# Optimization experiments

Measured on AMD Instinct MI355X. Metric: run time of the kernel, lower is better.

The kernel has to match this reference:

```python
import jax, jax.numpy as jnp
import numpy as np

D = 256; NH = 8; HD = D // NH; FF = 1024; NLAYERS = 6
REG_MAX = 32; NBIN = REG_MAX + 1; NC = 80; KQ = 4
SPATIAL = [(80, 80), (40, 40), (20, 20)]; NPTS = [4, 4, 4]; SUMP = sum(NPTS)
LQ = 300; B = 16; OFFSET_SCALE = 0.5; UP = 0.5; REG_SCALE = 4.0
TOT = NH * SUMP


def _project_np():
    ub1 = abs(UP) * abs(REG_SCALE); ub2 = ub1 * 2
    step = (ub1 + 1.0) ** (2.0 / (REG_MAX - 2))
    left = [-(step ** i) + 1 for i in range(REG_MAX // 2 - 1, 0, -1)]
    right = [step ** i - 1 for i in range(1, REG_MAX // 2)]
    return np.array([-ub2] + left + [0.0] + right + [ub2], dtype=np.float32)

PROJ_NP = _project_np()  # [NBIN]


def layer_norm(x, g, b):
    mu = x.mean(-1, keepdims=True)
    var = ((x - mu) ** 2).mean(-1, keepdims=True)
    return (x - mu) * jax.lax.rsqrt(var + 1e-5) * g + b


def inv_sigmoid(x, eps=1e-5):
    x = jnp.clip(x, eps, 1.0 - eps)
    return jnp.log(x) - jnp.log1p(-x)


def mlp2(x, w1, b1, w2, b2):
    return jax.nn.silu(x @ w1 + b1) @ w2 + b2


def mlp3(x, w1, b1, w2, b2, w3, b3):
    return jax.nn.silu(jax.nn.silu(x @ w1 + b1) @ w2 + b2) @ w3 + b3


def grid_sample(img, grid):
    # bilinear, padding_mode='zeros', align_corners=False. img [N,C,H,W], grid [N,Hg,Wg,2] in [-1,1]
    N, C, H, W = img.shape
    gshape = grid.shape[1:3]
    x = (grid[..., 0] + 1.0) * (W * 0.5) - 0.5
    y = (grid[..., 1] + 1.0) * (H * 0.5) - 0.5
    x0f = jnp.floor(x); y0f = jnp.floor(y)
    wx = x - x0f; wy = y - y0f
    x0 = x0f.astype(jnp.int32); y0 = y0f.astype(jnp.int32)
    imgf = img.reshape(N, C, H * W)
    def tap(xi, yi, wt):
        valid = ((xi >= 0) & (xi < W) & (yi >= 0) & (yi < H)).astype(img.dtype)
        idx = jnp.clip(yi, 0, H - 1) * W + jnp.clip(xi, 0, W - 1)
        v = jnp.take_along_axis(imgf, idx.reshape(N, 1, -1), axis=2).reshape(N, C, gshape[0], gshape[1])
        return v * (valid * wt)[:, None]
    return (tap(x0, y0, (1 - wx) * (1 - wy)) + tap(x0 + 1, y0, wx * (1 - wy))
            + tap(x0, y0 + 1, (1 - wx) * wy) + tap(x0 + 1, y0 + 1, wx * wy))


def self_attention(q_in, k_in, v_in, qw, qb, kw, kb, vw, vb, ow, ob):
    q = (q_in @ qw + qb).reshape(B, LQ, NH, HD)
    k = (k_in @ kw + kb).reshape(B, LQ, NH, HD)
    v = (v_in @ vw + vb).reshape(B, LQ, NH, HD)
    a = jax.nn.softmax(jnp.einsum('bqhd,bkhd->bhqk', q, k) * (HD ** -0.5), -1)
    o = jnp.einsum('bhqk,bkhd->bqhd', a, v).reshape(B, LQ, D)
    return o @ ow + ob


def distance2bbox(points, distance):
    rs = abs(REG_SCALE); half = 0.5 * rs
    x1 = points[..., 0] - (half + distance[..., 0]) * (points[..., 2] / rs)
    y1 = points[..., 1] - (half + distance[..., 1]) * (points[..., 3] / rs)
    x2 = points[..., 0] + (half + distance[..., 2]) * (points[..., 2] / rs)
    y2 = points[..., 1] + (half + distance[..., 3]) * (points[..., 3] / rs)
    return jnp.stack([(x1 + x2) * 0.5, (y1 + y2) * 0.5, x2 - x1, y2 - y1], -1)


def lqe_head(scores, corners, w1, b1, w2, b2):
    prob = jax.nn.softmax(corners.reshape(B, LQ, 4, NBIN), -1)
    topk, _ = jax.lax.top_k(prob, KQ)                         # [B,LQ,4,KQ]
    stat = jnp.concatenate([topk, topk.mean(-1, keepdims=True)], -1)  # [B,LQ,4,KQ+1]
    return scores + mlp2(stat.reshape(B, LQ, 4 * (KQ + 1)), w1, b1, w2, b2)


def reference(target, ref_pts_unact, memory,
              sa_qw, sa_qb, sa_kw, sa_kb, sa_vw, sa_vb, sa_ow, sa_ob,
              n1_g, n1_b, off_w, off_b, aw_w, aw_b,
              gate_w, gate_b, gn_g, gn_b,
              ff1_w, ff1_b, ff2_w, ff2_b, n3_g, n3_b,
              bb_w1, bb_b1, bb_w2, bb_b2, bb_w3, bb_b3,
              sc_w, sc_b, lqe_w1, lqe_b1, lqe_w2, lqe_b2,
              qp_w1, qp_b1, qp_w2, qp_b2,
              pb_w1, pb_b1, pb_w2, pb_b2, pb_w3, pb_b3):
    project = jnp.asarray(PROJ_NP)
    # --- value prep: memory [B,S,D] -> per-level [B*NH, HD, h, w] ---
    val = memory.reshape(B, -1, NH, HD).transpose(0, 2, 3, 1).reshape(B * NH, HD, -1)
    splits = np.cumsum([h * w for h, w in SPATIAL])[:-1].tolist()
    value_lvls = [v.reshape(B * NH, HD, h, w)
                  for v, (h, w) in zip(jnp.split(val, splits, axis=2), SPATIAL)]
    nps = jnp.asarray(np.repeat(1.0 / np.array(NPTS, np.float32), NPTS))  # [SUMP]

    ref_pts = jax.nn.sigmoid(ref_pts_unact)
    output = target
    out_prev = jnp.zeros_like(target)
    corners_prev = jnp.zeros((B, LQ, 4 * NBIN), dtype=target.dtype)
    ref_init = ref_pts
    final_logits = final_bboxes = None

    for i in range(NLAYERS):
        qp = jnp.clip(mlp2(ref_pts, qp_w1, qp_b1, qp_w2, qp_b2), -10.0, 10.0)
        # self attention
        q = output + qp
        t2 = self_attention(q, q, output, sa_qw[i], sa_qb[i], sa_kw[i], sa_kb[i],
                            sa_vw[i], sa_vb[i], sa_ow[i], sa_ob[i])
        output = layer_norm(output + t2, n1_g[i], n1_b[i])
        # deformable cross attention
        qc = output + qp
        offs = (qc @ off_w[i] + off_b[i]).reshape(B, LQ, NH, SUMP, 2)
        attnw = jax.nn.softmax((qc @ aw_w[i] + aw_b[i]).reshape(B, LQ, NH, SUMP), -1)
        offset = offs * nps[:, None] * ref_pts[:, :, None, None, 2:] * OFFSET_SCALE
        locs = ref_pts[:, :, None, None, :2] + offset            # [B,LQ,NH,SUMP,2]
        grids = (2.0 * locs - 1.0).transpose(0, 2, 1, 3, 4).reshape(B * NH, LQ, SUMP, 2)
        p0 = 0; sampled = []
        for lvl in range(len(SPATIAL)):
            sampled.append(grid_sample(value_lvls[lvl], grids[:, :, p0:p0 + NPTS[lvl]]))
            p0 += NPTS[lvl]
        samp = jnp.concatenate(sampled, -1)                      # [B*NH, HD, LQ, SUMP]
        aw = attnw.transpose(0, 2, 1, 3).reshape(B * NH, 1, LQ, SUMP)
        t2 = (samp * aw).sum(-1).reshape(B, D, LQ).transpose(0, 2, 1)
        # gateway
        g12 = jax.nn.sigmoid(jnp.concatenate([output, t2], -1) @ gate_w[i] + gate_b[i])
        output = layer_norm(g12[..., :D] * output + g12[..., D:] * t2, gn_g[i], gn_b[i])
        # FFN
        t2 = jax.nn.relu(output @ ff1_w[i] + ff1_b[i]) @ ff2_w[i] + ff2_b[i]
        output = layer_norm(jnp.clip(output + t2, -65504.0, 65504.0), n3_g[i], n3_b[i])
        # FDR box refinement
        if i == 0:
            pre_bb = jax.nn.sigmoid(mlp3(output, pb_w1, pb_b1, pb_w2, pb_b2, pb_w3, pb_b3)
                                    + inv_sigmoid(ref_pts))
            ref_init = pre_bb
        corners = mlp3(output + out_prev, bb_w1[i], bb_b1[i], bb_w2[i], bb_b2[i],
                       bb_w3[i], bb_b3[i]) + corners_prev
        dist = jax.nn.softmax(corners.reshape(B, LQ, 4, NBIN), -1) @ project  # [B,LQ,4]
        inter = distance2bbox(ref_init, dist)
        if i == NLAYERS - 1:  # eval_idx
            scores = output @ sc_w[i] + sc_b[i]
            final_logits = lqe_head(scores, corners, lqe_w1[i], lqe_b1[i], lqe_w2[i], lqe_b2[i])
            final_bboxes = inter
        corners_prev = corners
        ref_pts = inter
        out_prev = output
    return jnp.concatenate([final_bboxes, final_logits], -1)  # [B, LQ, 4+NC]


def setup_inputs() -> dict:
    key = jax.random.key(0)
    cnt = [0]
    def rnd(shape, scale=0.02):
        cnt[0] += 1
        return jax.random.normal(jax.random.fold_in(key, cnt[0]), shape, dtype=jnp.float32) * scale
    S = sum(h * w for h, w in SPATIAL)
    L = NLAYERS
    return {
        'target': rnd((B, LQ, D), 1.0),
        'ref_pts_unact': rnd((B, LQ, 4), 1.0),
        'memory': rnd((B, S, D), 1.0),
        'sa_qw': rnd((L, D, D)), 'sa_qb': rnd((L, D)),
        'sa_kw': rnd((L, D, D)), 'sa_kb': rnd((L, D)),
        'sa_vw': rnd((L, D, D)), 'sa_vb': rnd((L, D)),
        'sa_ow': rnd((L, D, D)), 'sa_ob': rnd((L, D)),
        'n1_g': jnp.ones((L, D)), 'n1_b': jnp.zeros((L, D)),
        'off_w': rnd((L, D, TOT * 2)), 'off_b': rnd((L, TOT * 2)),
        'aw_w': rnd((L, D, TOT)), 'aw_b': rnd((L, TOT)),
        'gate_w': rnd((L, 2 * D, 2 * D)), 'gate_b': rnd((L, 2 * D)),
        'gn_g': jnp.ones((L, D)), 'gn_b': jnp.zeros((L, D)),
        'ff1_w': rnd((L, D, FF)), 'ff1_b': rnd((L, FF)),
        'ff2_w': rnd((L, FF, D)), 'ff2_b': rnd((L, D)),
        'n3_g': jnp.ones((L, D)), 'n3_b': jnp.zeros((L, D)),
        'bb_w1': rnd((L, D, D)), 'bb_b1': rnd((L, D)),
        'bb_w2': rnd((L, D, D)), 'bb_b2': rnd((L, D)),
        'bb_w3': rnd((L, D, 4 * NBIN)), 'bb_b3': rnd((L, 4 * NBIN)),
        'sc_w': rnd((L, D, NC)), 'sc_b': rnd((L, NC)),
        'lqe_w1': rnd((L, 4 * (KQ + 1), 64)), 'lqe_b1': rnd((L, 64)),
        'lqe_w2': rnd((L, 64, 1)), 'lqe_b2': rnd((L, 1)),
        'qp_w1': rnd((4, 2 * D)), 'qp_b1': rnd((2 * D,)),
        'qp_w2': rnd((2 * D, D)), 'qp_b2': rnd((D,)),
        'pb_w1': rnd((D, D)), 'pb_b1': rnd((D,)),
        'pb_w2': rnd((D, D)), 'pb_b2': rnd((D,)),
        'pb_w3': rnd((D, 4)), 'pb_b3': rnd((4,)),
    }
```

## Files before the change

### kernel.cpp

```cpp
#include <hip/hip_runtime.h>
#include <cstddef>
#include <cmath>
#include <utility>

#define B_ 16
#define LQ_ 300
#define D_ 256
#define NH_ 8
#define HD_ 32
#define FF_ 1024
#define NBIN_ 33
#define NC_ 80
#define SUMP_ 12
#define TOT_ (NH_*SUMP_)
#define STOT_ 8400
#define R_ (B_*LQ_)
#define NLAYERS_ 6

typedef short bf16x8 __attribute__((ext_vector_type(8)));
typedef float f32x4  __attribute__((ext_vector_type(4)));

static __device__ __forceinline__ short f2bf(float x) {
  union { float f; unsigned u; } v; v.f = x;
  unsigned r = v.u + 0x7fffu + ((v.u >> 16) & 1u);
  return (short)(r >> 16);
}
static __device__ __forceinline__ float bf2f(short s) {
  union { unsigned u; float f; } v; v.u = ((unsigned)(unsigned short)s) << 16; return v.f;
}

__launch_bounds__(256)
__global__ void wconv_kernel(const float* __restrict__ W, short* __restrict__ Wt,
                             int K, int N, size_t ostride) {
  __shared__ float t[32][33];
  const float* Wl = W + (size_t)blockIdx.z * K * N;
  short* Wtl = Wt + (size_t)blockIdx.z * ostride;
  int k0 = blockIdx.x * 32, n0 = blockIdx.y * 32;
  int tr = threadIdx.x >> 5, tc = threadIdx.x & 31;
  #pragma unroll
  for (int i = 0; i < 4; ++i) {
    int k = k0 + tr + i * 8, n = n0 + tc;
    t[tr + i * 8][tc] = (k < K && n < N) ? Wl[(size_t)k * N + n] : 0.f;
  }
  __syncthreads();
  #pragma unroll
  for (int i = 0; i < 4; ++i) {
    int n = n0 + tr + i * 8, k = k0 + tc;
    if (n < N && k < K) Wtl[(size_t)n * K + k] = f2bf(t[tc][tr + i * 8]);
  }
}

__launch_bounds__(256)
__global__ void memconv_kernel(const float* __restrict__ mem, short* __restrict__ mb) {
  int gs = blockIdx.x * 4 + (threadIdx.x >> 6);
  int c  = (threadIdx.x & 63) * 4;
  int b = gs / STOT_, s = gs - b * STOT_;
  float4 v = *(const float4*)(mem + (size_t)gs * 256 + c);
  int h = c >> 5, cc = c & 31;
  short4 o; o.x = f2bf(v.x); o.y = f2bf(v.y); o.z = f2bf(v.z); o.w = f2bf(v.w);
  *(short4*)(mb + (((size_t)(b * 8 + h) * STOT_ + s) * 32) + cc) = o;
}

template<int ACT, int KT>
__launch_bounds__(256)
__global__ void bgemm(const short* __restrict__ A, const short* __restrict__ A2, int N2,
                      const short* __restrict__ Acat, int KA,
                      const short* __restrict__ Wt, const float* __restrict__ bias,
                      const float* __restrict__ Cadd, float* __restrict__ Cf,
                      short* __restrict__ Cbf, int M, int N) {
  const int bm = blockIdx.y * 64, bn = blockIdx.x * 64;
  const int tid = threadIdx.x, wid = tid >> 6, lane = tid & 63;
  const int wm = (wid >> 1) * 32, wn = (wid & 1) * 32;
  const int lr = lane & 15, lq = lane >> 4;
  const short* Ab = (A2 && bn >= N2) ? A2 : A;
  const int lda = Acat ? KA : KT;
  const int ldb = KT - KA;
  const int r0 = bm + wm + lr, r1 = r0 + 16;
  const int n0 = bn + wn + lr, n1 = n0 + 16;
  const bool v0 = n0 < N, v1 = n1 < N;
  const short* w0p = Wt + (size_t)(v0 ? n0 : 0) * KT + lq * 8;
  const short* w1p = Wt + (size_t)(v1 ? n1 : 0) * KT + lq * 8;
  f32x4 acc[2][2];
  #pragma unroll
  for (int i = 0; i < 2; ++i)
    #pragma unroll
    for (int j = 0; j < 2; ++j) acc[i][j] = (f32x4){0.f, 0.f, 0.f, 0.f};

  #pragma unroll 4
  for (int k0 = 0; k0 < KT; k0 += 32) {
    const short* src; int ko, ld;
    if (Acat && k0 >= KA) { src = Acat; ko = k0 - KA; ld = ldb; }
    else                  { src = Ab;   ko = k0;      ld = lda; }
    bf16x8 a0 = *(const bf16x8*)(src + (size_t)r0 * ld + ko + lq * 8);
    bf16x8 a1 = *(const bf16x8*)(src + (size_t)r1 * ld + ko + lq * 8);
    bf16x8 w0 = *(const bf16x8*)(w0p + k0);
    bf16x8 w1 = *(const bf16x8*)(w1p + k0);
    acc[0][0] = __builtin_amdgcn_mfma_f32_16x16x32_bf16(a0, w0, acc[0][0], 0, 0, 0);
    acc[0][1] = __builtin_amdgcn_mfma_f32_16x16x32_bf16(a0, w1, acc[0][1], 0, 0, 0);
    acc[1][0] = __builtin_amdgcn_mfma_f32_16x16x32_bf16(a1, w0, acc[1][0], 0, 0, 0);
    acc[1][1] = __builtin_amdgcn_mfma_f32_16x16x32_bf16(a1, w1, acc[1][1], 0, 0, 0);
  }
  #pragma unroll
  for (int ti = 0; ti < 2; ++ti)
    #pragma unroll
    for (int tj = 0; tj < 2; ++tj) {
      int gn = bn + wn + tj * 16 + lr;
      if (gn >= N) continue;
      float bv = bias[gn];
      #pragma unroll
      for (int r = 0; r < 4; ++r) {
        int gm = bm + wm + ti * 16 + lq * 4 + r;
        size_t idx = (size_t)gm * N + gn;
        float v = acc[ti][tj][r] + bv;
        if (Cadd) v += Cadd[idx];
        if (ACT == 1) v = fmaxf(v, 0.f);
        if (ACT == 2) v = v / (1.f + __expf(-v));
        if (ACT == 3) v = 1.f / (1.f + __expf(-v));
        if (ACT == 4) v = fminf(fmaxf(v, -10.f), 10.f);
        if (Cf)  Cf[idx] = v;
        if (Cbf) Cbf[idx] = f2bf(v);
      }
    }
}

template<int KT, int MODE>
__launch_bounds__(256)
__global__ void gemm_ln(const short* __restrict__ A, const short* __restrict__ Wt,
                        const float* __restrict__ bias, const float* __restrict__ resid,
                        const float* __restrict__ gamma, const float* __restrict__ beta,
                        const float* __restrict__ qp, float* __restrict__ prev,
                        float* __restrict__ outf, short* __restrict__ outbf,
                        short* __restrict__ oqbf) {
  __shared__ float ssum[16][4];
  __shared__ float ssq[16][4];
  const int m0 = blockIdx.x * 16;
  const int tid = threadIdx.x, wid = tid >> 6, lane = tid & 63;
  const int lr = lane & 15, lq = lane >> 4;
  const int arow = m0 + lr;
  const int cw = wid * 64;
  f32x4 acc[4];
  #pragma unroll
  for (int t = 0; t < 4; ++t) acc[t] = (f32x4){0.f, 0.f, 0.f, 0.f};
  #pragma unroll 4
  for (int k0 = 0; k0 < KT; k0 += 32) {
    bf16x8 a = *(const bf16x8*)(A + (size_t)arow * KT + k0 + lq * 8);
    #pragma unroll
    for (int t = 0; t < 4; ++t) {
      bf16x8 w = *(const bf16x8*)(Wt + (size_t)(cw + t * 16 + lr) * KT + k0 + lq * 8);
      acc[t] = __builtin_amdgcn_mfma_f32_16x16x32_bf16(a, w, acc[t], 0, 0, 0);
    }
  }
  float s[4] = {0.f, 0.f, 0.f, 0.f}, q[4] = {0.f, 0.f, 0.f, 0.f};
  #pragma unroll
  for (int t = 0; t < 4; ++t) {
    int col = cw + t * 16 + lr;
    float bv = bias[col];
    #pragma unroll
    for (int rr = 0; rr < 4; ++rr) {
      int rowg = m0 + lq * 4 + rr;
      float x = acc[t][rr] + bv + resid[(size_t)rowg * 256 + col];
      if (MODE == 1) x = fminf(fmaxf(x, -65504.f), 65504.f);
      acc[t][rr] = x;
      s[rr] += x; q[rr] += x * x;
    }
  }
  #pragma unroll
  for (int m = 1; m < 16; m <<= 1)
    #pragma unroll
    for (int rr = 0; rr < 4; ++rr) { s[rr] += __shfl_xor(s[rr], m); q[rr] += __shfl_xor(q[rr], m); }
  if (lr == 0)
    #pragma unroll
    for (int rr = 0; rr < 4; ++rr) {
      ssum[lq * 4 + rr][wid] = s[rr];
      ssq[lq * 4 + rr][wid] = q[rr];
    }
  __syncthreads();
  float mu[4], rs[4];
  #pragma unroll
  for (int rr = 0; rr < 4; ++rr) {
    int rl = lq * 4 + rr;
    float sm = ssum[rl][0] + ssum[rl][1] + ssum[rl][2] + ssum[rl][3];
    float sq = ssq[rl][0] + ssq[rl][1] + ssq[rl][2] + ssq[rl][3];
    float m_ = sm * (1.f / 256.f);
    float var = sq * (1.f / 256.f) - m_ * m_;
    mu[rr] = m_; rs[rr] = rsqrtf(var + 1e-5f);
  }
  #pragma unroll
  for (int t = 0; t < 4; ++t) {
    int col = cw + t * 16 + lr;
    float g = gamma[col], be = beta[col];
    #pragma unroll
    for (int rr = 0; rr < 4; ++rr) {
      int rowg = m0 + lq * 4 + rr;
      size_t idx = (size_t)rowg * 256 + col;
      float v = (acc[t][rr] - mu[rr]) * rs[rr] * g + be;
      outf[idx] = v;
      outbf[idx] = f2bf(v);
      if (MODE == 0) {
        oqbf[idx] = f2bf(v + qp[idx]);
      } else {
        float po = prev[idx];
        oqbf[idx] = f2bf(v + po);
        prev[idx] = v;
      }
    }
  }
}

__launch_bounds__(256)
__global__ void ffn_ln(const short* __restrict__ A, const short* __restrict__ W1t,
                       const float* __restrict__ b1, const short* __restrict__ W2t,
                       const float* __restrict__ b2, const float* __restrict__ resid,
                       const float* __restrict__ gamma, const float* __restrict__ beta,
                       float* __restrict__ prev, float* __restrict__ outf,
                       short* __restrict__ outbf, short* __restrict__ oqbf) {
  __shared__ short hid[16][1032];
  __shared__ float ssum[16][4];
  __shared__ float ssq[16][4];
  const int m0 = blockIdx.x * 16;
  const int tid = threadIdx.x, wid = tid >> 6, lane = tid & 63;
  const int lr = lane & 15, lq = lane >> 4;
  const int arow = m0 + lr;
  {
    f32x4 acc[16];
    #pragma unroll
    for (int t = 0; t < 16; ++t) acc[t] = (f32x4){0.f, 0.f, 0.f, 0.f};
    #pragma unroll 2
    for (int k0 = 0; k0 < 256; k0 += 32) {
      bf16x8 a = *(const bf16x8*)(A + (size_t)arow * 256 + k0 + lq * 8);
      #pragma unroll
      for (int t = 0; t < 16; ++t) {
        bf16x8 w = *(const bf16x8*)(W1t + (size_t)(wid * 256 + t * 16 + lr) * 256 + k0 + lq * 8);
        acc[t] = __builtin_amdgcn_mfma_f32_16x16x32_bf16(a, w, acc[t], 0, 0, 0);
      }
    }
    #pragma unroll
    for (int t = 0; t < 16; ++t) {
      int col = wid * 256 + t * 16 + lr;
      float bv = b1[col];
      #pragma unroll
      for (int rr = 0; rr < 4; ++rr)
        hid[lq * 4 + rr][col] = f2bf(fmaxf(acc[t][rr] + bv, 0.f));
    }
  }
  __syncthreads();
  const int cw = wid * 64;
  f32x4 acc[4];
  #pragma unroll
  for (int t = 0; t < 4; ++t) acc[t] = (f32x4){0.f, 0.f, 0.f, 0.f};
  #pragma unroll 4
  for (int k0 = 0; k0 < 1024; k0 += 32) {
    bf16x8 a = *(const bf16x8*)&hid[lr][k0 + lq * 8];
    #pragma unroll
    for (int t = 0; t < 4; ++t) {
      bf16x8 w = *(const bf16x8*)(W2t + (size_t)(cw + t * 16 + lr) * 1024 + k0 + lq * 8);
      acc[t] = __builtin_amdgcn_mfma_f32_16x16x32_bf16(a, w, acc[t], 0, 0, 0);
    }
  }
  float s[4] = {0.f, 0.f, 0.f, 0.f}, q[4] = {0.f, 0.f, 0.f, 0.f};
  #pragma unroll
  for (int t = 0; t < 4; ++t) {
    int col = cw + t * 16 + lr;
    float bv = b2[col];
    #pragma unroll
    for (int rr = 0; rr < 4; ++rr) {
      int rowg = m0 + lq * 4 + rr;
      float x = acc[t][rr] + bv + resid[(size_t)rowg * 256 + col];
      x = fminf(fmaxf(x, -65504.f), 65504.f);
      acc[t][rr] = x;
      s[rr] += x; q[rr] += x * x;
    }
  }
  #pragma unroll
  for (int m = 1; m < 16; m <<= 1)
    #pragma unroll
    for (int rr = 0; rr < 4; ++rr) { s[rr] += __shfl_xor(s[rr], m); q[rr] += __shfl_xor(q[rr], m); }
  if (lr == 0)
    #pragma unroll
    for (int rr = 0; rr < 4; ++rr) {
      ssum[lq * 4 + rr][wid] = s[rr];
      ssq[lq * 4 + rr][wid] = q[rr];
    }
  __syncthreads();
  float mu[4], rs[4];
  #pragma unroll
  for (int rr = 0; rr < 4; ++rr) {
    int rl = lq * 4 + rr;
    float sm = ssum[rl][0] + ssum[rl][1] + ssum[rl][2] + ssum[rl][3];
    float sq = ssq[rl][0] + ssq[rl][1] + ssq[rl][2] + ssq[rl][3];
    float m_ = sm * (1.f / 256.f);
    float var = sq * (1.f / 256.f) - m_ * m_;
    mu[rr] = m_; rs[rr] = rsqrtf(var + 1e-5f);
  }
  #pragma unroll
  for (int t = 0; t < 4; ++t) {
    int col = cw + t * 16 + lr;
    float g = gamma[col], be = beta[col];
    #pragma unroll
    for (int rr = 0; rr < 4; ++rr) {
      int rowg = m0 + lq * 4 + rr;
      size_t idx = (size_t)rowg * 256 + col;
      float v = (acc[t][rr] - mu[rr]) * rs[rr] * g + be;
      outf[idx] = v;
      outbf[idx] = f2bf(v);
      float po = prev[idx];
      oqbf[idx] = f2bf(v + po);
      prev[idx] = v;
    }
  }
}

__launch_bounds__(256)
__global__ void fdr_kernel(const short* __restrict__ A,
                           const short* __restrict__ W1t, const float* __restrict__ b1,
                           const short* __restrict__ W2t, const float* __restrict__ b2,
                           const short* __restrict__ W3t, const float* __restrict__ b3,
                           const float* __restrict__ cprev, const float* __restrict__ refi,
                           float* __restrict__ ccur, float* __restrict__ refn) {
  __shared__ short h1[16][264];
  __shared__ short h2[16][264];
  __shared__ float cor[16][132];
  __shared__ float dstl[16][4];
  __shared__ float projs[33];
  const int m0 = blockIdx.x * 16;
  const int tid = threadIdx.x, wid = tid >> 6, lane = tid & 63;
  const int lr = lane & 15, lq = lane >> 4;
  if (tid < 33) {
    float v;
    if (tid == 0) v = -4.f;
    else if (tid == 32) v = 4.f;
    else if (tid == 16) v = 0.f;
    else if (tid < 16) v = 1.f - powf(3.f, (float)(16 - tid) * (1.f / 15.f));
    else v = powf(3.f, (float)(tid - 16) * (1.f / 15.f)) - 1.f;
    projs[tid] = v;
  }
  {
    f32x4 acc[4];
    #pragma unroll
    for (int t = 0; t < 4; ++t) acc[t] = (f32x4){0.f, 0.f, 0.f, 0.f};
    #pragma unroll 2
    for (int k0 = 0; k0 < 256; k0 += 32) {
      bf16x8 a = *(const bf16x8*)(A + (size_t)(m0 + lr) * 256 + k0 + lq * 8);
      #pragma unroll
      for (int t = 0; t < 4; ++t) {
        bf16x8 w = *(const bf16x8*)(W1t + (size_t)(wid * 64 + t * 16 + lr) * 256 + k0 + lq * 8);
        acc[t] = __builtin_amdgcn_mfma_f32_16x16x32_bf16(a, w, acc[t], 0, 0, 0);
      }
    }
    #pragma unroll
    for (int t = 0; t < 4; ++t) {
      int col = wid * 64 + t * 16 + lr;
      float bv = b1[col];
      #pragma unroll
      for (int rr = 0; rr < 4; ++rr) {
        float v = acc[t][rr] + bv;
        v = v / (1.f + __expf(-v));
        h1[lq * 4 + rr][col] = f2bf(v);
      }
    }
  }
  __syncthreads();
  {
    f32x4 acc[4];
    #pragma unroll
    for (int t = 0; t < 4; ++t) acc[t] = (f32x4){0.f, 0.f, 0.f, 0.f};
    #pragma unroll 2
    for (int k0 = 0; k0 < 256; k0 += 32) {
      bf16x8 a = *(const bf16x8*)&h1[lr][k0 + lq * 8];
      #pragma unroll
      for (int t = 0; t < 4; ++t) {
        bf16x8 w = *(const bf16x8*)(W2t + (size_t)(wid * 64 + t * 16 + lr) * 256 + k0 + lq * 8);
        acc[t] = __builtin_amdgcn_mfma_f32_16x16x32_bf16(a, w, acc[t], 0, 0, 0);
      }
    }
    #pragma unroll
    for (int t = 0; t < 4; ++t) {
      int col = wid * 64 + t * 16 + lr;
      float bv = b2[col];
      #pragma unroll
      for (int rr = 0; rr < 4; ++rr) {
        float v = acc[t][rr] + bv;
        v = v / (1.f + __expf(-v));
        h2[lq * 4 + rr][col] = f2bf(v);
      }
    }
  }
  __syncthreads();
  {
    f32x4 acc[3];
    int col[3], wr[3];
    #pragma unroll
    for (int j = 0; j < 3; ++j) {
      acc[j] = (f32x4){0.f, 0.f, 0.f, 0.f};
      col[j] = (wid + j * 4) * 16 + lr;
      wr[j] = (col[j] < 132) ? col[j] : 0;
    }
    #pragma unroll 2
    for (int k0 = 0; k0 < 256; k0 += 32) {
      bf16x8 a = *(const bf16x8*)&h2[lr][k0 + lq * 8];
      #pragma unroll
      for (int j = 0; j < 3; ++j) {
        bf16x8 w = *(const bf16x8*)(W3t + (size_t)wr[j] * 256 + k0 + lq * 8);
        acc[j] = __builtin_amdgcn_mfma_f32_16x16x32_bf16(a, w, acc[j], 0, 0, 0);
      }
    }
    #pragma unroll
    for (int j = 0; j < 3; ++j) {
      if (col[j] >= 132) continue;
      float bv = b3[col[j]];
      #pragma unroll
      for (int rr = 0; rr < 4; ++rr) {
        int rl = lq * 4 + rr, g = m0 + rl;
        float v = acc[j][rr] + bv + cprev[(size_t)g * 132 + col[j]];
        ccur[(size_t)g * 132 + col[j]] = v;
        cor[rl][col[j]] = v;
      }
    }
  }
  __syncthreads();
  if (tid < 64) {
    int r = tid >> 2, sd = tid & 3;
    const float* cp = &cor[r][sd * 33];
    float m = -1e30f;
    #pragma unroll
    for (int j = 0; j < 33; ++j) m = fmaxf(m, cp[j]);
    float sum = 0.f, dot = 0.f;
    #pragma unroll
    for (int j = 0; j < 33; ++j) { float e = __expf(cp[j] - m); sum += e; dot += e * projs[j]; }
    dstl[r][sd] = dot / sum;
  }
  __syncthreads();
  if (tid < 16) {
    int g = m0 + tid;
    float px = refi[g * 4], py = refi[g * 4 + 1];
    float qw = refi[g * 4 + 2] * 0.25f, qh = refi[g * 4 + 3] * 0.25f;
    float x1 = px - (2.f + dstl[tid][0]) * qw, y1 = py - (2.f + dstl[tid][1]) * qh;
    float x2 = px + (2.f + dstl[tid][2]) * qw, y2 = py + (2.f + dstl[tid][3]) * qh;
    float4 o; o.x = (x1 + x2) * 0.5f; o.y = (y1 + y2) * 0.5f; o.z = x2 - x1; o.w = y2 - y1;
    *(float4*)(refn + (size_t)g * 4) = o;
  }
}

__launch_bounds__(256)
__global__ void pb_fused(const short* __restrict__ A,
                         const short* __restrict__ W1t, const float* __restrict__ b1,
                         const short* __restrict__ W2t, const float* __restrict__ b2,
                         const short* __restrict__ W3t, const float* __restrict__ b3,
                         const float* __restrict__ refc, float* __restrict__ refinit) {
  __shared__ short h1[16][264];
  __shared__ short h2[16][264];
  const int m0 = blockIdx.x * 16;
  const int tid = threadIdx.x, wid = tid >> 6, lane = tid & 63;
  const int lr = lane & 15, lq = lane >> 4;
  {
    f32x4 acc[4];
    #pragma unroll
    for (int t = 0; t < 4; ++t) acc[t] = (f32x4){0.f, 0.f, 0.f, 0.f};
    #pragma unroll 2
    for (int k0 = 0; k0 < 256; k0 += 32) {
      bf16x8 a = *(const bf16x8*)(A + (size_t)(m0 + lr) * 256 + k0 + lq * 8);
      #pragma unroll
      for (int t = 0; t < 4; ++t) {
        bf16x8 w = *(const bf16x8*)(W1t + (size_t)(wid * 64 + t * 16 + lr) * 256 + k0 + lq * 8);
        acc[t] = __builtin_amdgcn_mfma_f32_16x16x32_bf16(a, w, acc[t], 0, 0, 0);
      }
    }
    #pragma unroll
    for (int t = 0; t < 4; ++t) {
      int col = wid * 64 + t * 16 + lr;
      float bv = b1[col];
      #pragma unroll
      for (int rr = 0; rr < 4; ++rr) {
        float v = acc[t][rr] + bv;
        v = v / (1.f + __expf(-v));
        h1[lq * 4 + rr][col] = f2bf(v);
      }
    }
  }
  __syncthreads();
  {
    f32x4 acc[4];
    #pragma unroll
    for (int t = 0; t < 4; ++t) acc[t] = (f32x4){0.f, 0.f, 0.f, 0.f};
    #pragma unroll 2
    for (int k0 = 0; k0 < 256; k0 += 32) {
      bf16x8 a = *(const bf16x8*)&h1[lr][k0 + lq * 8];
      #pragma unroll
      for (int t = 0; t < 4; ++t) {
        bf16x8 w = *(const bf16x8*)(W2t + (size_t)(wid * 64 + t * 16 + lr) * 256 + k0 + lq * 8);
        acc[t] = __builtin_amdgcn_mfma_f32_16x16x32_bf16(a, w, acc[t], 0, 0, 0);
      }
    }
    #pragma unroll
    for (int t = 0; t < 4; ++t) {
      int col = wid * 64 + t * 16 + lr;
      float bv = b2[col];
      #pragma unroll
      for (int rr = 0; rr < 4; ++rr) {
        float v = acc[t][rr] + bv;
        v = v / (1.f + __expf(-v));
        h2[lq * 4 + rr][col] = f2bf(v);
      }
    }
  }
  __syncthreads();
  if (wid == 0) {
    f32x4 acc = (f32x4){0.f, 0.f, 0.f, 0.f};
    const short* wp = W3t + (size_t)((lr < 4) ? lr : 0) * 256;
    #pragma unroll 2
    for (int k0 = 0; k0 < 256; k0 += 32) {
      bf16x8 a = *(const bf16x8*)&h2[lr][k0 + lq * 8];
      bf16x8 w = *(const bf16x8*)(wp + k0 + lq * 8);
      acc = __builtin_amdgcn_mfma_f32_16x16x32_bf16(a, w, acc, 0, 0, 0);
    }
    if (lr < 4) {
      float bv = b3[lr];
      #pragma unroll
      for (int rr = 0; rr < 4; ++rr) {
        int g = m0 + lq * 4 + rr;
        float pre = acc[rr] + bv;
        float x = fminf(fmaxf(refc[(size_t)g * 4 + lr], 1e-5f), 1.f - 1e-5f);
        float is = logf(x) - log1pf(-x);
        refinit[(size_t)g * 4 + lr] = 1.f / (1.f + __expf(-(pre + is)));
      }
    }
  }
}

__launch_bounds__(256)
__global__ void gate_ln(const short* __restrict__ Abf, const short* __restrict__ tbf,
                        const short* __restrict__ Wt, const float* __restrict__ bias,
                        const float* __restrict__ t2,
                        const float* __restrict__ gamma, const float* __restrict__ beta,
                        float* __restrict__ output, short* __restrict__ outbf) {
  __shared__ float sg[16][520];
  const int m0 = blockIdx.x * 16;
  const int tid = threadIdx.x, wid = tid >> 6, lane = tid & 63;
  const int lr = lane & 15, lq = lane >> 4;
  const int arow = m0 + lr;
  f32x4 acc[8];
  #pragma unroll
  for (int t = 0; t < 8; ++t) acc[t] = (f32x4){0.f, 0.f, 0.f, 0.f};
  #pragma unroll 2
  for (int k0 = 0; k0 < 512; k0 += 32) {
    const short* src = (k0 < 256) ? Abf : tbf;
    int ko = (k0 < 256) ? k0 : k0 - 256;
    bf16x8 a = *(const bf16x8*)(src + (size_t)arow * 256 + ko + lq * 8);
    #pragma unroll
    for (int t = 0; t < 8; ++t) {
      bf16x8 w = *(const bf16x8*)(Wt + (size_t)(wid * 128 + t * 16 + lr) * 512 + k0 + lq * 8);
      acc[t] = __builtin_amdgcn_mfma_f32_16x16x32_bf16(a, w, acc[t], 0, 0, 0);
    }
  }
  #pragma unroll
  for (int t = 0; t < 8; ++t) {
    int col = wid * 128 + t * 16 + lr;
    float bv = bias[col];
    #pragma unroll
    for (int rr = 0; rr < 4; ++rr) {
      int rl = lq * 4 + rr;
      sg[rl][col] = 1.f / (1.f + __expf(-(acc[t][rr] + bv)));
    }
  }
  __syncthreads();
  #pragma unroll
  for (int it = 0; it < 4; ++it) {
    int rl = wid + it * 4;
    int rowg = m0 + rl;
    int c = lane * 4;
    float4 o4 = *(const float4*)(output + (size_t)rowg * 256 + c);
    float4 t4 = *(const float4*)(t2 + (size_t)rowg * 256 + c);
    float4 g1 = *(const float4*)&sg[rl][c];
    float4 g2 = *(const float4*)&sg[rl][256 + c];
    float x0 = g1.x * o4.x + g2.x * t4.x;
    float x1 = g1.y * o4.y + g2.y * t4.y;
    float x2 = g1.z * o4.z + g2.z * t4.z;
    float x3 = g1.w * o4.w + g2.w * t4.w;
    float s = x0 + x1 + x2 + x3;
    float q = x0 * x0 + x1 * x1 + x2 * x2 + x3 * x3;
    #pragma unroll
    for (int o = 32; o; o >>= 1) { s += __shfl_xor(s, o); q += __shfl_xor(q, o); }
    float mu = s * (1.f / 256.f);
    float var = q * (1.f / 256.f) - mu * mu;
    float rs = rsqrtf(var + 1e-5f);
    float4 ga = *(const float4*)(gamma + c);
    float4 be = *(const float4*)(beta + c);
    float v0 = (x0 - mu) * rs * ga.x + be.x;
    float v1 = (x1 - mu) * rs * ga.y + be.y;
    float v2 = (x2 - mu) * rs * ga.z + be.z;
    float v3 = (x3 - mu) * rs * ga.w + be.w;
    float4 vo; vo.x = v0; vo.y = v1; vo.z = v2; vo.w = v3;
    *(float4*)(output + (size_t)rowg * 256 + c) = vo;
    short4 vs; vs.x = f2bf(v0); vs.y = f2bf(v1); vs.z = f2bf(v2); vs.w = f2bf(v3);
    *(short4*)(outbf + (size_t)rowg * 256 + c) = vs;
  }
}

__launch_bounds__(256)
__global__ void qp_mlp(const float* __restrict__ ref, const float* __restrict__ W1,
                       const float* __restrict__ b1, const short* __restrict__ W2t,
                       const float* __restrict__ b2, const float* __restrict__ output,
                       float* __restrict__ qpout, short* __restrict__ oqbf) {
  __shared__ short sh[16 * 520];
  const int m0 = blockIdx.x * 16;
  const int tid = threadIdx.x;
  for (int i = tid; i < 16 * 512; i += 256) {
    int r = i >> 9, n = i & 511;
    float4 rv = *(const float4*)(ref + (size_t)(m0 + r) * 4);
    float v = b1[n] + rv.x * W1[n] + rv.y * W1[512 + n] + rv.z * W1[1024 + n]
            + rv.w * W1[1536 + n];
    v = v / (1.f + __expf(-v));
    sh[r * 520 + n] = f2bf(v);
  }
  __syncthreads();
  const int wid = tid >> 6, lane = tid & 63;
  const int lr = lane & 15, lq = lane >> 4;
  f32x4 acc[4];
  #pragma unroll
  for (int t = 0; t < 4; ++t) acc[t] = (f32x4){0.f, 0.f, 0.f, 0.f};
  #pragma unroll 4
  for (int k0 = 0; k0 < 512; k0 += 32) {
    bf16x8 a = *(const bf16x8*)&sh[lr * 520 + k0 + lq * 8];
    #pragma unroll
    for (int t = 0; t < 4; ++t) {
      bf16x8 w = *(const bf16x8*)(W2t + (size_t)(wid * 64 + t * 16 + lr) * 512 + k0 + lq * 8);
      acc[t] = __builtin_amdgcn_mfma_f32_16x16x32_bf16(a, w, acc[t], 0, 0, 0);
    }
  }
  #pragma unroll
  for (int t = 0; t < 4; ++t) {
    int col = wid * 64 + t * 16 + lr;
    float bv = b2[col];
    #pragma unroll
    for (int rr = 0; rr < 4; ++rr) {
      int rowg = m0 + lq * 4 + rr;
      size_t idx = (size_t)rowg * 256 + col;
      float v = fminf(fmaxf(acc[t][rr] + bv, -10.f), 10.f);
      qpout[idx] = v;
      oqbf[idx] = f2bf(v + output[idx]);
    }
  }
}

__launch_bounds__(256)
__global__ void attn3_kernel(const short* __restrict__ qkv, short* __restrict__ O) {
  __shared__ short Kb[304][40];
  __shared__ short Vt[32][328];
  __shared__ short Pw[4][16][328];
  const int half = blockIdx.x & 1, bh = blockIdx.x >> 1;
  const int h = bh & 7, b = bh >> 3;
  const int tid = threadIdx.x;
  const short* QKVb = qkv + (size_t)b * LQ_ * 768;
  for (int idx = tid; idx < 304 * 4; idx += 256) {
    int row = idx >> 2, seg = (idx & 3) * 8;
    bf16x8 v = (row < 300) ? *(const bf16x8*)(QKVb + (size_t)row * 768 + 256 + h * 32 + seg)
                           : (bf16x8){0,0,0,0,0,0,0,0};
    *(bf16x8*)&Kb[row][seg] = v;
  }
  for (int idx = tid; idx < 300 * 4; idx += 256) {
    int row = idx >> 2, seg = (idx & 3) * 8;
    bf16x8 v = *(const bf16x8*)(QKVb + (size_t)row * 768 + 512 + h * 32 + seg);
    #pragma unroll
    for (int j = 0; j < 8; ++j) Vt[seg + j][row] = v[j];
  }
  for (int idx = tid; idx < 32 * 20; idx += 256) Vt[idx / 20][300 + idx % 20] = 0;
  for (int idx = tid; idx < 4 * 16 * 16; idx += 256)
    Pw[idx >> 8][(idx >> 4) & 15][304 + (idx & 15)] = 0;
  __syncthreads();

  const int wid = tid >> 6, lane = tid & 63;
  const int lr = lane & 15, lq = lane >> 4;
  short (*Pl)[328] = Pw[wid];
  const float scale = 0.17677669529663687f;

  for (int qt = wid; qt < 10; qt += 4) {
    const int q0 = half * 150 + qt * 16;
    int qrow = q0 + lr; if (qrow > 299) qrow = 299;
    bf16x8 af_q = *(const bf16x8*)(QKVb + (size_t)qrow * 768 + h * 32 + lq * 8);
    f32x4 s[19];
    #pragma unroll
    for (int t = 0; t < 19; ++t) {
      bf16x8 bk = *(const bf16x8*)&Kb[t * 16 + lr][lq * 8];
      s[t] = __builtin_amdgcn_mfma_f32_16x16x32_bf16(af_q, bk, (f32x4){0.f,0.f,0.f,0.f}, 0, 0, 0);
    }
    #pragma unroll
    for (int t = 0; t < 19; ++t)
      #pragma unroll
      for (int r = 0; r < 4; ++r) s[t][r] *= scale;
    if (lr >= 12) { s[18][0] = s[18][1] = s[18][2] = s[18][3] = -1e30f; }
    float l[4];
    #pragma unroll
    for (int r = 0; r < 4; ++r) {
      float mm = -1e30f;
      #pragma unroll
      for (int t = 0; t < 19; ++t) mm = fmaxf(mm, s[t][r]);
      #pragma unroll
      for (int x = 1; x < 16; x <<= 1) mm = fmaxf(mm, __shfl_xor(mm, x));
      float ll = 0.f;
      #pragma unroll
      for (int t = 0; t < 19; ++t) { float p = __expf(s[t][r] - mm); s[t][r] = p; ll += p; }
      #pragma unroll
      for (int x = 1; x < 16; x <<= 1) ll += __shfl_xor(ll, x);
      l[r] = ll;
    }
    #pragma unroll
    for (int t = 0; t < 19; ++t)
      #pragma unroll
      for (int r = 0; r < 4; ++r) Pl[lq * 4 + r][t * 16 + lr] = f2bf(s[t][r]);
    f32x4 o0 = (f32x4){0.f,0.f,0.f,0.f}, o1 = (f32x4){0.f,0.f,0.f,0.f};
    #pragma unroll
    for (int c = 0; c < 10; ++c) {
      bf16x8 ap = *(const bf16x8*)&Pl[lr][c * 32 + lq * 8];
      bf16x8 v0 = *(const bf16x8*)&Vt[lr][c * 32 + lq * 8];
      bf16x8 v1 = *(const bf16x8*)&Vt[16 + lr][c * 32 + lq * 8];
      o0 = __builtin_amdgcn_mfma_f32_16x16x32_bf16(ap, v0, o0, 0, 0, 0);
      o1 = __builtin_amdgcn_mfma_f32_16x16x32_bf16(ap, v1, o1, 0, 0, 0);
    }
    #pragma unroll
    for (int r = 0; r < 4; ++r) {
      int q = q0 + lq * 4 + r;
      if (q >= 300) continue;
      float inv = 1.f / l[r];
      size_t ob = (size_t)(b * LQ_ + q) * 256 + h * 32;
      O[ob + lr]      = f2bf(o0[r] * inv);
      O[ob + 16 + lr] = f2bf(o1[r] * inv);
    }
  }
}

template<int BF16MEM>
__launch_bounds__(256)
__global__ void deform_kernel(const void* __restrict__ memv, const float* __restrict__ offaw,
                              const float* __restrict__ refp,
                              float* __restrict__ t2, short* __restrict__ t2bf) {
  const int bi = blockIdx.x;
  const int row = (bi & 7) * 600 + (bi >> 3);
  const int b = row / LQ_;
  const int tid = threadIdx.x;
  const int h = tid >> 5, c = tid & 31;
  const float rx = refp[row * 4 + 0], ry = refp[row * 4 + 1];
  const float rw = refp[row * 4 + 2], rh = refp[row * 4 + 3];
  const float* awp = offaw + (size_t)row * 288 + 192 + h * SUMP_;
  float wv[SUMP_];
  float wmax = -1e30f;
  #pragma unroll
  for (int p = 0; p < SUMP_; ++p) { wv[p] = awp[p]; wmax = fmaxf(wmax, wv[p]); }
  float wsum = 0.f;
  #pragma unroll
  for (int p = 0; p < SUMP_; ++p) { wv[p] = __expf(wv[p] - wmax); wsum += wv[p]; }
  const float winv = 1.f / wsum;
  const float* op = offaw + (size_t)row * 288 + h * (SUMP_ * 2);
  const short* mb16 = BF16MEM ? ((const short*)memv + ((size_t)(b * 8 + h) * STOT_) * 32 + c) : nullptr;
  const float* mb32 = BF16MEM ? nullptr : ((const float*)memv + (size_t)b * STOT_ * 256 + h * 32 + c);
  float acc = 0.f;
  #pragma unroll
  for (int p = 0; p < SUMP_; ++p) {
    const int lvl = p >> 2;
    const int Wl = (lvl == 0) ? 80 : ((lvl == 1) ? 40 : 20);
    const int s0 = (lvl == 0) ? 0 : ((lvl == 1) ? 6400 : 8000);
    float lx = rx + op[2 * p]     * 0.125f * rw;
    float ly = ry + op[2 * p + 1] * 0.125f * rh;
    float x = lx * Wl - 0.5f, y = ly * Wl - 0.5f;
    float xf = floorf(x), yf = floorf(y);
    int x0 = (int)xf, y0 = (int)yf;
    float wx = x - xf, wy = y - yf;
    int x0c = min(max(x0, 0), Wl - 1), x1c = min(max(x0 + 1, 0), Wl - 1);
    int y0c = min(max(y0, 0), Wl - 1), y1c = min(max(y0 + 1, 0), Wl - 1);
    float wx0 = (x0 >= 0 && x0 < Wl) ? (1.f - wx) : 0.f;
    float wx1 = (x0 + 1 >= 0 && x0 + 1 < Wl) ? wx : 0.f;
    float wy0 = (y0 >= 0 && y0 < Wl) ? (1.f - wy) : 0.f;
    float wy1 = (y0 + 1 >= 0 && y0 + 1 < Wl) ? wy : 0.f;
    float v;
    if (BF16MEM) {
      const short* mb = mb16 + (size_t)s0 * 32;
      v = wx0 * wy0 * bf2f(mb[(size_t)(y0c * Wl + x0c) * 32])
        + wx1 * wy0 * bf2f(mb[(size_t)(y0c * Wl + x1c) * 32])
        + wx0 * wy1 * bf2f(mb[(size_t)(y1c * Wl + x0c) * 32])
        + wx1 * wy1 * bf2f(mb[(size_t)(y1c * Wl + x1c) * 32]);
    } else {
      const float* mb = mb32 + (size_t)s0 * 256;
      v = wx0 * wy0 * mb[(size_t)(y0c * Wl + x0c) * 256]
        + wx1 * wy0 * mb[(size_t)(y0c * Wl + x1c) * 256]
        + wx0 * wy1 * mb[(size_t)(y1c * Wl + x0c) * 256]
        + wx1 * wy1 * mb[(size_t)(y1c * Wl + x1c) * 256];
    }
    acc += wv[p] * winv * v;
  }
  size_t off = (size_t)row * D_ + h * HD_ + c;
  t2[off] = acc;
  t2bf[off] = f2bf(acc);
}

__launch_bounds__(64)
__global__ void lqe_kernel(const float* __restrict__ scores, const float* __restrict__ corners,
                           const float* __restrict__ w1, const float* __restrict__ b1,
                           const float* __restrict__ w2, const float* __restrict__ b2,
                           const float* __restrict__ inter, float* __restrict__ out) {
  const int row = blockIdx.x;
  const int tid = threadIdx.x;
  __shared__ float stat[20];
  __shared__ float lqe_s;
  if (tid < 4) {
    const float* cp = corners + (size_t)row * (4 * NBIN_) + tid * NBIN_;
    float m = -1e30f;
    for (int j = 0; j < NBIN_; ++j) m = fmaxf(m, cp[j]);
    float e[NBIN_]; float sum = 0.f;
    for (int j = 0; j < NBIN_; ++j) { e[j] = __expf(cp[j] - m); sum += e[j]; }
    float inv = 1.f / sum;
    float mean = 0.f;
    for (int t = 0; t < 4; ++t) {
      int bi = 0; float best = -1.f;
      for (int j = 0; j < NBIN_; ++j) if (e[j] > best) { best = e[j]; bi = j; }
      e[bi] = -2.f;
      float v = best * inv;
      stat[tid * 5 + t] = v; mean += v;
    }
    stat[tid * 5 + 4] = mean * 0.25f;
  }
  __syncthreads();
  float s = b1[tid];
  #pragma unroll
  for (int i = 0; i < 20; ++i) s += stat[i] * w1[i * 64 + tid];
  float hv = s / (1.f + __expf(-s));
  float v = hv * w2[tid];
  #pragma unroll
  for (int o = 32; o; o >>= 1) v += __shfl_down(v, o);
  if (tid == 0) lqe_s = v + b2[0];
  __syncthreads();
  if (tid < 4) out[(size_t)row * 84 + tid] = inter[row * 4 + tid];
  for (int c = tid; c < NC_; c += 64)
    out[(size_t)row * 84 + 4 + c] = scores[(size_t)row * NC_ + c] + lqe_s;
}

__global__ void fill0_kernel(float* __restrict__ p, int n) {
  int i = blockIdx.x * 256 + threadIdx.x; if (i < n) p[i] = 0.f;
}
__global__ void sigmoid_kernel(float* __restrict__ d, const float* __restrict__ s, int n) {
  int i = blockIdx.x * 256 + threadIdx.x; if (i < n) d[i] = 1.f / (1.f + __expf(-s[i]));
}
__global__ void initcvt_kernel(float* __restrict__ o, short* __restrict__ ob,
                               const float* __restrict__ t, int n4) {
  int i = blockIdx.x * 256 + threadIdx.x;
  if (i < n4) {
    float4 v = ((const float4*)t)[i];
    ((float4*)o)[i] = v;
    short4 s; s.x = f2bf(v.x); s.y = f2bf(v.y); s.z = f2bf(v.z); s.w = f2bf(v.w);
    ((short4*)ob)[i] = s;
  }
}
__global__ void bcat_kernel(const float* __restrict__ qb, const float* __restrict__ kb,
                            const float* __restrict__ vb, const float* __restrict__ ob,
                            const float* __restrict__ ab, float* __restrict__ qkvb,
                            float* __restrict__ offawb) {
  int i = blockIdx.x * 256 + threadIdx.x;
  if (i < NLAYERS_ * 768) {
    int l = i / 768, c = i % 768;
    qkvb[i] = (c < 256) ? qb[l * 256 + c] : (c < 512) ? kb[l * 256 + c - 256]
                        : vb[l * 256 + c - 512];
  }
  if (i < NLAYERS_ * 288) {
    int l = i / 288, c = i % 288;
    offawb[i] = (c < 192) ? ob[l * 192 + c] : ab[l * 96 + c - 192];
  }
}

template<int KT>
static void launch_bgemm_k(hipStream_t st, const short* A, const short* A2, int N2,
                           const short* Acat, int KA, const short* Wt, const float* bias,
                           const float* Cadd, float* Cf, short* Cbf, int M, int N, int act) {
  dim3 g((N + 63) / 64, M / 64), blk(256);
  switch (act) {
    case 0: bgemm<0,KT><<<g, blk, 0, st>>>(A, A2, N2, Acat, KA, Wt, bias, Cadd, Cf, Cbf, M, N); break;
    case 1: bgemm<1,KT><<<g, blk, 0, st>>>(A, A2, N2, Acat, KA, Wt, bias, Cadd, Cf, Cbf, M, N); break;
    case 2: bgemm<2,KT><<<g, blk, 0, st>>>(A, A2, N2, Acat, KA, Wt, bias, Cadd, Cf, Cbf, M, N); break;
    case 3: bgemm<3,KT><<<g, blk, 0, st>>>(A, A2, N2, Acat, KA, Wt, bias, Cadd, Cf, Cbf, M, N); break;
    case 4: bgemm<4,KT><<<g, blk, 0, st>>>(A, A2, N2, Acat, KA, Wt, bias, Cadd, Cf, Cbf, M, N); break;
  }
}
static void launch_bgemm(hipStream_t st, const short* A, const short* A2, int N2,
                         const short* Acat, int KA, const short* Wt, const float* bias,
                         const float* Cadd, float* Cf, short* Cbf,
                         int M, int N, int K, int act) {
  if (K == 256)      launch_bgemm_k<256>(st, A, A2, N2, Acat, KA, Wt, bias, Cadd, Cf, Cbf, M, N, act);
  else if (K == 512) launch_bgemm_k<512>(st, A, A2, N2, Acat, KA, Wt, bias, Cadd, Cf, Cbf, M, N, act);
  else               launch_bgemm_k<1024>(st, A, A2, N2, Acat, KA, Wt, bias, Cadd, Cf, Cbf, M, N, act);
}

static void conv_w(hipStream_t st, const float* W, short* Wt, int K, int N, int L,
                   size_t ostride) {
  dim3 g((K + 31) / 32, (N + 31) / 32, L);
  wconv_kernel<<<g, 256, 0, st>>>(W, Wt, K, N, ostride);
}

static inline dim3 egrid(int n) { return dim3((n + 255) / 256); }

extern "C" void kernel_launch(void* const* d_in, const int* in_sizes, int n_in,
                              void* d_out, int out_size, void* d_ws, size_t ws_size,
                              hipStream_t stream) {
  const float* target     = (const float*)d_in[0];
  const float* ref_unact  = (const float*)d_in[1];
  const float* memory     = (const float*)d_in[2];
  const float* sa_qw = (const float*)d_in[3];  const float* sa_qb = (const float*)d_in[4];
  const float* sa_kw = (const float*)d_in[5];  const float* sa_kb = (const float*)d_in[6];
  const float* sa_vw = (const float*)d_in[7];  const float* sa_vb = (const float*)d_in[8];
  const float* sa_ow = (const float*)d_in[9];  const float* sa_ob = (const float*)d_in[10];
  const float* n1_g  = (const float*)d_in[11]; const float* n1_b  = (const float*)d_in[12];
  const float* off_w = (const float*)d_in[13]; const float* off_b = (const float*)d_in[14];
  const float* aw_w  = (const float*)d_in[15]; const float* aw_b  = (const float*)d_in[16];
  const float* gate_w= (const float*)d_in[17]; const float* gate_b= (const float*)d_in[18];
  const float* gn_g  = (const float*)d_in[19]; const float* gn_b  = (const float*)d_in[20];
  const float* ff1_w = (const float*)d_in[21]; const float* ff1_b = (const float*)d_in[22];
  const float* ff2_w = (const float*)d_in[23]; const float* ff2_b = (const float*)d_in[24];
  const float* n3_g  = (const float*)d_in[25]; const float* n3_b  = (const float*)d_in[26];
  const float* bb_w1 = (const float*)d_in[27]; const float* bb_b1 = (const float*)d_in[28];
  const float* bb_w2 = (const float*)d_in[29]; const float* bb_b2 = (const float*)d_in[30];
  const float* bb_w3 = (const float*)d_in[31]; const float* bb_b3 = (const float*)d_in[32];
  const float* sc_w  = (const float*)d_in[33]; const float* sc_b  = (const float*)d_in[34];
  const float* lqe_w1= (const float*)d_in[35]; const float* lqe_b1= (const float*)d_in[36];
  const float* lqe_w2= (const float*)d_in[37]; const float* lqe_b2= (const float*)d_in[38];
  const float* qp_w1 = (const float*)d_in[39]; const float* qp_b1 = (const float*)d_in[40];
  const float* qp_w2 = (const float*)d_in[41]; const float* qp_b2 = (const float*)d_in[42];
  const float* pb_w1 = (const float*)d_in[43]; const float* pb_b1 = (const float*)d_in[44];
  const float* pb_w2 = (const float*)d_in[45]; const float* pb_b2 = (const float*)d_in[46];
  const float* pb_w3 = (const float*)d_in[47]; const float* pb_b3 = (const float*)d_in[48];
  float* out = (float*)d_out;

  float* ws = (float*)d_ws;
  size_t woff = 0;
  auto alloc = [&](size_t n) { float* p = ws + woff; woff += n; return p; };
  float* output   = alloc((size_t)R_ * D_);
  float* out_prev = alloc((size_t)R_ * D_);
  float* qp       = alloc((size_t)R_ * D_);
  float* t2       = alloc((size_t)R_ * D_);
  float* offawf   = alloc((size_t)R_ * 288);
  float* U        = alloc((size_t)R_ * 512);
  float* corners0 = alloc((size_t)R_ * 4 * NBIN_);
  float* corners1 = alloc((size_t)R_ * 4 * NBIN_);
  float* refA     = alloc((size_t)R_ * 4);
  float* refB     = alloc((size_t)R_ * 4);
  float* ref_init = alloc((size_t)R_ * 4);
  float* qkvb     = alloc((size_t)NLAYERS_ * 768);
  float* offawb   = alloc((size_t)NLAYERS_ * 288);

  short* sws = (short*)(ws + woff);
  size_t soff = 0;
  auto salloc = [&](size_t n) { short* p = sws + soff; soff += n; return p; };
  short* outbf = salloc((size_t)R_ * D_);
  short* oqbf  = salloc((size_t)R_ * D_);
  short* tbf   = salloc((size_t)R_ * D_);
  short* qp2t  = salloc((size_t)256 * 512);
  short* sqkvt = salloc((size_t)NLAYERS_ * 768 * 256);
  short* sowt  = salloc((size_t)NLAYERS_ * 256 * 256);
  short* soffawt = salloc((size_t)NLAYERS_ * 288 * 256);
  short* gatet = salloc((size_t)NLAYERS_ * 512 * 512);
  short* ff1t  = salloc((size_t)NLAYERS_ * 1024 * 256);
  short* ff2t  = salloc((size_t)NLAYERS_ * 256 * 1024);
  short* bb1t  = salloc((size_t)NLAYERS_ * 256 * 256);
  short* bb2t  = salloc((size_t)NLAYERS_ * 256 * 256);
  short* bb3t  = salloc((size_t)NLAYERS_ * 132 * 256);
  short* pb1t  = salloc((size_t)256 * 256);
  short* pb2t  = salloc((size_t)256 * 256);
  short* pb3t  = salloc((size_t)4 * 256);
  short* sct   = salloc((size_t)80 * 256);
  size_t base_bytes = woff * sizeof(float) + soff * sizeof(short);
  if (ws_size < base_bytes) return;
  const size_t memn = (size_t)B_ * STOT_ * 256;
  bool bf16mem = (ws_size >= base_bytes + memn * sizeof(short));
  short* membf = sws + soff;

  short* qkv    = (short*)U;
  float* scores = offawf;

  float* c_prev = corners0; float* c_cur = corners1;
  float* ref_cur = refA;    float* ref_nxt = refB;

  conv_w(stream, qp_w2, qp2t, 512, 256, 1, 0);
  conv_w(stream, sa_qw, sqkvt,               256, 256, NLAYERS_, 768 * 256);
  conv_w(stream, sa_kw, sqkvt + 256 * 256,   256, 256, NLAYERS_, 768 * 256);
  conv_w(stream, sa_vw, sqkvt + 512 * 256,   256, 256, NLAYERS_, 768 * 256);
  conv_w(stream, sa_ow, sowt, 256, 256, NLAYERS_, 256 * 256);
  conv_w(stream, off_w, soffawt,             256, 192, NLAYERS_, 288 * 256);
  conv_w(stream, aw_w,  soffawt + 192 * 256, 256,  96, NLAYERS_, 288 * 256);
  conv_w(stream, gate_w, gatet, 512, 512, NLAYERS_, 512 * 512);
  conv_w(stream, ff1_w, ff1t, 256, 1024, NLAYERS_, 1024 * 256);
  conv_w(stream, ff2_w, ff2t, 1024, 256, NLAYERS_, 256 * 1024);
  conv_w(stream, bb_w1, bb1t, 256, 256, NLAYERS_, 256 * 256);
  conv_w(stream, bb_w2, bb2t, 256, 256, NLAYERS_, 256 * 256);
  conv_w(stream, bb_w3, bb3t, 256, 132, NLAYERS_, 132 * 256);
  conv_w(stream, pb_w1, pb1t, 256, 256, 1, 0);
  conv_w(stream, pb_w2, pb2t, 256, 256, 1, 0);
  conv_w(stream, pb_w3, pb3t, 256, 4, 1, 0);
  conv_w(stream, sc_w + (size_t)5 * D_ * NC_, sct, 256, 80, 1, 0);
  bcat_kernel<<<egrid(NLAYERS_ * 768), 256, 0, stream>>>(sa_qb, sa_kb, sa_vb, off_b, aw_b,
                                                         qkvb, offawb);
  if (bf16mem)
    memconv_kernel<<<dim3(B_ * STOT_ / 4), 256, 0, stream>>>(memory, membf);

  fill0_kernel<<<egrid(R_ * D_), 256, 0, stream>>>(out_prev, R_ * D_);
  fill0_kernel<<<egrid(R_ * 4 * NBIN_), 256, 0, stream>>>(c_prev, R_ * 4 * NBIN_);
  sigmoid_kernel<<<egrid(R_ * 4), 256, 0, stream>>>(ref_cur, ref_unact, R_ * 4);
  initcvt_kernel<<<egrid(R_ * D_ / 4), 256, 0, stream>>>(output, outbf, target, R_ * D_ / 4);

  for (int i = 0; i < NLAYERS_; ++i) {
    qp_mlp<<<dim3(300), 256, 0, stream>>>(ref_cur, qp_w1, qp_b1, qp2t, qp_b2,
                                          output, qp, oqbf);

    launch_bgemm(stream, oqbf, outbf, 512, nullptr, 0, sqkvt + (size_t)i * 768 * 256,
                 qkvb + (size_t)i * 768, nullptr, nullptr, qkv, R_, 768, 256, 0);
    attn3_kernel<<<dim3(B_ * NH_ * 2), 256, 0, stream>>>(qkv, tbf);
    gemm_ln<256, 0><<<dim3(300), 256, 0, stream>>>(
        tbf, sowt + (size_t)i * 65536, sa_ob + (size_t)i * D_, output,
        n1_g + (size_t)i * D_, n1_b + (size_t)i * D_, qp, nullptr,
        output, outbf, oqbf);

    launch_bgemm(stream, oqbf, nullptr, 0, nullptr, 0, soffawt + (size_t)i * 288 * 256,
                 offawb + (size_t)i * 288, nullptr, offawf, nullptr, R_, 288, 256, 0);
    if (bf16mem)
      deform_kernel<1><<<dim3(R_), 256, 0, stream>>>(membf, offawf, ref_cur, t2, tbf);
    else
      deform_kernel<0><<<dim3(R_), 256, 0, stream>>>(memory, offawf, ref_cur, t2, tbf);

    gate_ln<<<dim3(300), 256, 0, stream>>>(outbf, tbf, gatet + (size_t)i * 262144,
                                           gate_b + (size_t)i * 512, t2,
                                           gn_g + (size_t)i * D_, gn_b + (size_t)i * D_,
                                           output, outbf);

    ffn_ln<<<dim3(300), 256, 0, stream>>>(outbf, ff1t + (size_t)i * 262144,
                                          ff1_b + (size_t)i * FF_,
                                          ff2t + (size_t)i * 262144, ff2_b + (size_t)i * D_,
                                          output, n3_g + (size_t)i * D_, n3_b + (size_t)i * D_,
                                          out_prev, output, outbf, oqbf);

    if (i == 0)
      pb_fused<<<dim3(300), 256, 0, stream>>>(outbf, pb1t, pb_b1, pb2t, pb_b2,
                                              pb3t, pb_b3, ref_cur, ref_init);
    fdr_kernel<<<dim3(300), 256, 0, stream>>>(oqbf,
                                              bb1t + (size_t)i * 65536, bb_b1 + (size_t)i * D_,
                                              bb2t + (size_t)i * 65536, bb_b2 + (size_t)i * D_,
                                              bb3t + (size_t)i * 33792, bb_b3 + (size_t)i * 4 * NBIN_,
                                              c_prev, ref_init, c_cur, ref_nxt);

    if (i == NLAYERS_ - 1) {
      launch_bgemm(stream, outbf, nullptr, 0, nullptr, 0, sct, sc_b + (size_t)5 * NC_,
                   nullptr, scores, nullptr, R_, NC_, 256, 0);
      lqe_kernel<<<dim3(R_), 64, 0, stream>>>(scores, c_cur,
                                              lqe_w1 + (size_t)5 * 20 * 64, lqe_b1 + (size_t)5 * 64,
                                              lqe_w2 + (size_t)5 * 64, lqe_b2 + (size_t)5,
                                              ref_nxt, out);
    } else {
      std::swap(c_prev, c_cur);
      std::swap(ref_cur, ref_nxt);
    }
  }
}
```

Measured before the change: 1.947 ms.

## Fuse per-layer GEMMs into neighbouring kernels and batch weight conversion into one launch

The weight transpose/convert launches become a single job-table kernel, and the init fills, sigmoid and bias concatenation are merged into one kernel. The query-pos MLP is fused with the QKV projection, the sampling-offset GEMM is folded into the attention-output LayerNorm kernel, and the final score GEMM and LQE head are fused into the FFN and distribution kernels. The aim is to cut launch count and round trips of intermediates through global memory. The cost is heavier fused kernels with more registers and shared memory and lower parallelism per fused GEMM, since each block handles only 16 rows over the full output width.

```diff
diff --git a/kernel.cpp b/kernel.cpp
--- a/kernel.cpp
+++ b/kernel.cpp
@@ -29,13 +29,25 @@
   union { unsigned u; float f; } v; v.u = ((unsigned)(unsigned short)s) << 16; return v.f;
 }
 
+struct WJob { const float* src; short* dst; int K, N, tk, tn, L, ostride, blk0, pad; };
+struct WJobs { WJob j[17]; int njobs; };
+
 __launch_bounds__(256)
-__global__ void wconv_kernel(const float* __restrict__ W, short* __restrict__ Wt,
-                             int K, int N, size_t ostride) {
+__global__ void wconv_all(WJobs P) {
   __shared__ float t[32][33];
-  const float* Wl = W + (size_t)blockIdx.z * K * N;
-  short* Wtl = Wt + (size_t)blockIdx.z * ostride;
-  int k0 = blockIdx.x * 32, n0 = blockIdx.y * 32;
+  const int b = blockIdx.x;
+  int ji = 0;
+  for (int k = 1; k < P.njobs; ++k) ji = (b >= P.j[k].blk0) ? k : ji;
+  const float* src = P.j[ji].src;
+  short* dst = P.j[ji].dst;
+  const int K = P.j[ji].K, N = P.j[ji].N, tk = P.j[ji].tk;
+  int rel = b - P.j[ji].blk0;
+  int per = tk * P.j[ji].tn;
+  int l = rel / per; int r2 = rel - l * per;
+  int tki = r2 % tk, tni = r2 / tk;
+  const float* Wl = src + (size_t)l * K * N;
+  short* Wtl = dst + (size_t)l * (size_t)P.j[ji].ostride;
+  int k0 = tki * 32, n0 = tni * 32;
   int tr = threadIdx.x >> 5, tc = threadIdx.x & 31;
   #pragma unroll
   for (int i = 0; i < 4; ++i) {
@@ -61,78 +73,132 @@
   *(short4*)(mb + (((size_t)(b * 8 + h) * STOT_ + s) * 32) + cc) = o;
 }
 
-template<int ACT, int KT>
 __launch_bounds__(256)
-__global__ void bgemm(const short* __restrict__ A, const short* __restrict__ A2, int N2,
-                      const short* __restrict__ Acat, int KA,
-                      const short* __restrict__ Wt, const float* __restrict__ bias,
-                      const float* __restrict__ Cadd, float* __restrict__ Cf,
-                      short* __restrict__ Cbf, int M, int N) {
-  const int bm = blockIdx.y * 64, bn = blockIdx.x * 64;
-  const int tid = threadIdx.x, wid = tid >> 6, lane = tid & 63;
-  const int wm = (wid >> 1) * 32, wn = (wid & 1) * 32;
+__global__ void misc_init(const float* __restrict__ target, const float* __restrict__ refu,
+                          const float* __restrict__ qb, const float* __restrict__ kb,
+                          const float* __restrict__ vb, const float* __restrict__ ob,
+                          const float* __restrict__ ab,
+                          float* __restrict__ output, short* __restrict__ outbf,
+                          float* __restrict__ out_prev, float* __restrict__ cprev,
+                          float* __restrict__ refcur, float* __restrict__ qkvb,
+                          float* __restrict__ offawb) {
+  int i = blockIdx.x * 256 + threadIdx.x;
+  float4 z; z.x = 0.f; z.y = 0.f; z.z = 0.f; z.w = 0.f;
+  if (i < R_ * 64) {
+    float4 v = ((const float4*)target)[i];
+    ((float4*)output)[i] = v;
+    short4 s; s.x = f2bf(v.x); s.y = f2bf(v.y); s.z = f2bf(v.z); s.w = f2bf(v.w);
+    ((short4*)outbf)[i] = s;
+    ((float4*)out_prev)[i] = z;
+  }
+  if (i < R_ * 33) ((float4*)cprev)[i] = z;
+  if (i < R_) {
+    float4 r = ((const float4*)refu)[i];
+    float4 o;
+    o.x = 1.f / (1.f + __expf(-r.x)); o.y = 1.f / (1.f + __expf(-r.y));
+    o.z = 1.f / (1.f + __expf(-r.z)); o.w = 1.f / (1.f + __expf(-r.w));
+    ((float4*)refcur)[i] = o;
+  }
+  if (i < NLAYERS_ * 768) {
+    int l = i / 768, c = i % 768;
+    qkvb[i] = (c < 256) ? qb[l * 256 + c] : (c < 512) ? kb[l * 256 + c - 256]
+                        : vb[l * 256 + c - 512];
+  }
+  if (i < NLAYERS_ * 288) {
+    int l = i / 288, c = i % 288;
+    offawb[i] = (c < 192) ? ob[l * 192 + c] : ab[l * 96 + c - 192];
+  }
+}
+
+__launch_bounds__(256)
+__global__ void qp_qkv(const float* __restrict__ ref, const float* __restrict__ W1,
+                       const float* __restrict__ b1, const short* __restrict__ W2t,
+                       const float* __restrict__ b2, const float* __restrict__ output,
+                       const short* __restrict__ outbf,
+                       const short* __restrict__ Qt, const float* __restrict__ qkvbias,
+                       float* __restrict__ qpout, short* __restrict__ qkvout) {
+  __shared__ short sh[16 * 520];
+  __shared__ short oqs[16][264];
+  const int m0 = blockIdx.x * 16;
+  const int tid = threadIdx.x;
+  for (int i = tid; i < 16 * 512; i += 256) {
+    int r = i >> 9, n = i & 511;
+    float4 rv = *(const float4*)(ref + (size_t)(m0 + r) * 4);
+    float v = b1[n] + rv.x * W1[n] + rv.y * W1[512 + n] + rv.z * W1[1024 + n]
+            + rv.w * W1[1536 + n];
+    v = v / (1.f + __expf(-v));
+    sh[r * 520 + n] = f2bf(v);
+  }
+  __syncthreads();
+  const int wid = tid >> 6, lane = tid & 63;
   const int lr = lane & 15, lq = lane >> 4;
-  const short* Ab = (A2 && bn >= N2) ? A2 : A;
-  const int lda = Acat ? KA : KT;
-  const int ldb = KT - KA;
-  const int r0 = bm + wm + lr, r1 = r0 + 16;
-  const int n0 = bn + wn + lr, n1 = n0 + 16;
-  const bool v0 = n0 < N, v1 = n1 < N;
-  const short* w0p = Wt + (size_t)(v0 ? n0 : 0) * KT + lq * 8;
-  const short* w1p = Wt + (size_t)(v1 ? n1 : 0) * KT + lq * 8;
-  f32x4 acc[2][2];
-  #pragma unroll
-  for (int i = 0; i < 2; ++i)
-    #pragma unroll
-    for (int j = 0; j < 2; ++j) acc[i][j] = (f32x4){0.f, 0.f, 0.f, 0.f};
-
-  #pragma unroll 4
-  for (int k0 = 0; k0 < KT; k0 += 32) {
-    const short* src; int ko, ld;
-    if (Acat && k0 >= KA) { src = Acat; ko = k0 - KA; ld = ldb; }
-    else                  { src = Ab;   ko = k0;      ld = lda; }
-    bf16x8 a0 = *(const bf16x8*)(src + (size_t)r0 * ld + ko + lq * 8);
-    bf16x8 a1 = *(const bf16x8*)(src + (size_t)r1 * ld + ko + lq * 8);
-    bf16x8 w0 = *(const bf16x8*)(w0p + k0);
-    bf16x8 w1 = *(const bf16x8*)(w1p + k0);
-    acc[0][0] = __builtin_amdgcn_mfma_f32_16x16x32_bf16(a0, w0, acc[0][0], 0, 0, 0);
-    acc[0][1] = __builtin_amdgcn_mfma_f32_16x16x32_bf16(a0, w1, acc[0][1], 0, 0, 0);
-    acc[1][0] = __builtin_amdgcn_mfma_f32_16x16x32_bf16(a1, w0, acc[1][0], 0, 0, 0);
-    acc[1][1] = __builtin_amdgcn_mfma_f32_16x16x32_bf16(a1, w1, acc[1][1], 0, 0, 0);
-  }
-  #pragma unroll
-  for (int ti = 0; ti < 2; ++ti)
-    #pragma unroll
-    for (int tj = 0; tj < 2; ++tj) {
-      int gn = bn + wn + tj * 16 + lr;
-      if (gn >= N) continue;
-      float bv = bias[gn];
-      #pragma unroll
-      for (int r = 0; r < 4; ++r) {
-        int gm = bm + wm + ti * 16 + lq * 4 + r;
-        size_t idx = (size_t)gm * N + gn;
-        float v = acc[ti][tj][r] + bv;
-        if (Cadd) v += Cadd[idx];
-        if (ACT == 1) v = fmaxf(v, 0.f);
-        if (ACT == 2) v = v / (1.f + __expf(-v));
-        if (ACT == 3) v = 1.f / (1.f + __expf(-v));
-        if (ACT == 4) v = fminf(fmaxf(v, -10.f), 10.f);
-        if (Cf)  Cf[idx] = v;
-        if (Cbf) Cbf[idx] = f2bf(v);
-      }
-    }
-}
-
-template<int KT, int MODE>
+  {
+    f32x4 acc[4];
+    #pragma unroll
+    for (int t = 0; t < 4; ++t) acc[t] = (f32x4){0.f, 0.f, 0.f, 0.f};
+    #pragma unroll 4
+    for (int k0 = 0; k0 < 512; k0 += 32) {
+      bf16x8 a = *(const bf16x8*)&sh[lr * 520 + k0 + lq * 8];
+      #pragma unroll
+      for (int t = 0; t < 4; ++t) {
+        bf16x8 w = *(const bf16x8*)(W2t + (size_t)(wid * 64 + t * 16 + lr) * 512 + k0 + lq * 8);
+        acc[t] = __builtin_amdgcn_mfma_f32_16x16x32_bf16(a, w, acc[t], 0, 0, 0);
+      }
+    }
+    #pragma unroll
+    for (int t = 0; t < 4; ++t) {
+      int col = wid * 64 + t * 16 + lr;
+      float bv = b2[col];
+      #pragma unroll
+      for (int rr = 0; rr < 4; ++rr) {
+        int rl = lq * 4 + rr;
+        size_t idx = (size_t)(m0 + rl) * 256 + col;
+        float v = fminf(fmaxf(acc[t][rr] + bv, -10.f), 10.f);
+        qpout[idx] = v;
+        oqs[rl][col] = f2bf(v + output[idx]);
+      }
+    }
+  }
+  __syncthreads();
+  {
+    f32x4 acc[12];
+    #pragma unroll
+    for (int t = 0; t < 12; ++t) acc[t] = (f32x4){0.f, 0.f, 0.f, 0.f};
+    const int cbase = wid * 192;
+    const short* obp = outbf + (size_t)(m0 + lr) * 256;
+    #pragma unroll 2
+    for (int k0 = 0; k0 < 256; k0 += 32) {
+      bf16x8 a_oq = *(const bf16x8*)&oqs[lr][k0 + lq * 8];
+      bf16x8 a_ob = *(const bf16x8*)(obp + k0 + lq * 8);
+      #pragma unroll
+      for (int t = 0; t < 12; ++t) {
+        bf16x8 w = *(const bf16x8*)(Qt + (size_t)(cbase + t * 16 + lr) * 256 + k0 + lq * 8);
+        acc[t] = __builtin_amdgcn_mfma_f32_16x16x32_bf16(
+            (cbase + t * 16 < 512) ? a_oq : a_ob, w, acc[t], 0, 0, 0);
+      }
+    }
+    #pragma unroll
+    for (int t = 0; t < 12; ++t) {
+      int colt = cbase + t * 16 + lr;
+      float bv = qkvbias[colt];
+      #pragma unroll
+      for (int rr = 0; rr < 4; ++rr)
+        qkvout[(size_t)(m0 + lq * 4 + rr) * 768 + colt] = f2bf(acc[t][rr] + bv);
+    }
+  }
+}
+
 __launch_bounds__(256)
-__global__ void gemm_ln(const short* __restrict__ A, const short* __restrict__ Wt,
-                        const float* __restrict__ bias, const float* __restrict__ resid,
-                        const float* __restrict__ gamma, const float* __restrict__ beta,
-                        const float* __restrict__ qp, float* __restrict__ prev,
-                        float* __restrict__ outf, short* __restrict__ outbf,
-                        short* __restrict__ oqbf) {
+__global__ void sow_ln_off(const short* __restrict__ A, const short* __restrict__ Wt,
+                           const float* __restrict__ bias, const float* __restrict__ resid,
+                           const float* __restrict__ gamma, const float* __restrict__ beta,
+                           const float* __restrict__ qp,
+                           const short* __restrict__ OWt, const float* __restrict__ ob,
+                           float* __restrict__ outf, short* __restrict__ outbf,
+                           float* __restrict__ offout) {
   __shared__ float ssum[16][4];
   __shared__ float ssq[16][4];
+  __shared__ short oqs[16][264];
   const int m0 = blockIdx.x * 16;
   const int tid = threadIdx.x, wid = tid >> 6, lane = tid & 63;
   const int lr = lane & 15, lq = lane >> 4;
@@ -142,11 +208,11 @@
   #pragma unroll
   for (int t = 0; t < 4; ++t) acc[t] = (f32x4){0.f, 0.f, 0.f, 0.f};
   #pragma unroll 4
-  for (int k0 = 0; k0 < KT; k0 += 32) {
-    bf16x8 a = *(const bf16x8*)(A + (size_t)arow * KT + k0 + lq * 8);
+  for (int k0 = 0; k0 < 256; k0 += 32) {
+    bf16x8 a = *(const bf16x8*)(A + (size_t)arow * 256 + k0 + lq * 8);
     #pragma unroll
     for (int t = 0; t < 4; ++t) {
-      bf16x8 w = *(const bf16x8*)(Wt + (size_t)(cw + t * 16 + lr) * KT + k0 + lq * 8);
+      bf16x8 w = *(const bf16x8*)(Wt + (size_t)(cw + t * 16 + lr) * 256 + k0 + lq * 8);
       acc[t] = __builtin_amdgcn_mfma_f32_16x16x32_bf16(a, w, acc[t], 0, 0, 0);
     }
   }
@@ -159,7 +225,6 @@
     for (int rr = 0; rr < 4; ++rr) {
       int rowg = m0 + lq * 4 + rr;
       float x = acc[t][rr] + bv + resid[(size_t)rowg * 256 + col];
-      if (MODE == 1) x = fminf(fmaxf(x, -65504.f), 65504.f);
       acc[t][rr] = x;
       s[rr] += x; q[rr] += x * x;
     }
@@ -191,29 +256,51 @@
     float g = gamma[col], be = beta[col];
     #pragma unroll
     for (int rr = 0; rr < 4; ++rr) {
-      int rowg = m0 + lq * 4 + rr;
-      size_t idx = (size_t)rowg * 256 + col;
+      int rl = lq * 4 + rr;
+      size_t idx = (size_t)(m0 + rl) * 256 + col;
       float v = (acc[t][rr] - mu[rr]) * rs[rr] * g + be;
       outf[idx] = v;
       outbf[idx] = f2bf(v);
-      if (MODE == 0) {
-        oqbf[idx] = f2bf(v + qp[idx]);
-      } else {
-        float po = prev[idx];
-        oqbf[idx] = f2bf(v + po);
-        prev[idx] = v;
-      }
-    }
-  }
-}
-
+      oqs[rl][col] = f2bf(v + qp[idx]);
+    }
+  }
+  __syncthreads();
+  f32x4 oacc[5];
+  #pragma unroll
+  for (int j = 0; j < 5; ++j) oacc[j] = (f32x4){0.f, 0.f, 0.f, 0.f};
+  #pragma unroll 2
+  for (int k0 = 0; k0 < 256; k0 += 32) {
+    bf16x8 a = *(const bf16x8*)&oqs[lr][k0 + lq * 8];
+    #pragma unroll
+    for (int j = 0; j < 5; ++j) {
+      int tile = wid + j * 4;
+      int trow = (tile < 18) ? tile * 16 + lr : 0;
+      bf16x8 w = *(const bf16x8*)(OWt + (size_t)trow * 256 + k0 + lq * 8);
+      oacc[j] = __builtin_amdgcn_mfma_f32_16x16x32_bf16(a, w, oacc[j], 0, 0, 0);
+    }
+  }
+  #pragma unroll
+  for (int j = 0; j < 5; ++j) {
+    int tile = wid + j * 4;
+    if (tile >= 18) continue;
+    int col = tile * 16 + lr;
+    float bv = ob[col];
+    #pragma unroll
+    for (int rr = 0; rr < 4; ++rr)
+      offout[(size_t)(m0 + lq * 4 + rr) * 288 + col] = oacc[j][rr] + bv;
+  }
+}
+
+template<int SCORES>
 __launch_bounds__(256)
 __global__ void ffn_ln(const short* __restrict__ A, const short* __restrict__ W1t,
                        const float* __restrict__ b1, const short* __restrict__ W2t,
                        const float* __restrict__ b2, const float* __restrict__ resid,
                        const float* __restrict__ gamma, const float* __restrict__ beta,
                        float* __restrict__ prev, float* __restrict__ outf,
-                       short* __restrict__ outbf, short* __restrict__ oqbf) {
+                       short* __restrict__ outbf, short* __restrict__ oqbf,
+                       const short* __restrict__ SCt, const float* __restrict__ scb,
+                       float* __restrict__ scoresOut) {
   __shared__ short hid[16][1032];
   __shared__ float ssum[16][4];
   __shared__ float ssq[16][4];
@@ -298,30 +385,66 @@
     float g = gamma[col], be = beta[col];
     #pragma unroll
     for (int rr = 0; rr < 4; ++rr) {
-      int rowg = m0 + lq * 4 + rr;
-      size_t idx = (size_t)rowg * 256 + col;
+      int rl = lq * 4 + rr;
+      size_t idx = (size_t)(m0 + rl) * 256 + col;
       float v = (acc[t][rr] - mu[rr]) * rs[rr] * g + be;
       outf[idx] = v;
-      outbf[idx] = f2bf(v);
+      short vb = f2bf(v);
+      outbf[idx] = vb;
       float po = prev[idx];
       oqbf[idx] = f2bf(v + po);
       prev[idx] = v;
-    }
-  }
-}
-
+      if (SCORES) hid[rl][col] = vb;
+    }
+  }
+  if (SCORES) {
+    __syncthreads();
+    f32x4 sacc[2];
+    sacc[0] = (f32x4){0.f, 0.f, 0.f, 0.f};
+    sacc[1] = (f32x4){0.f, 0.f, 0.f, 0.f};
+    #pragma unroll 2
+    for (int k0 = 0; k0 < 256; k0 += 32) {
+      bf16x8 a = *(const bf16x8*)&hid[lr][k0 + lq * 8];
+      #pragma unroll
+      for (int j = 0; j < 2; ++j) {
+        int tile = wid + j * 4;
+        int trow = (tile < 5) ? tile * 16 + lr : 0;
+        bf16x8 w = *(const bf16x8*)(SCt + (size_t)trow * 256 + k0 + lq * 8);
+        sacc[j] = __builtin_amdgcn_mfma_f32_16x16x32_bf16(a, w, sacc[j], 0, 0, 0);
+      }
+    }
+    #pragma unroll
+    for (int j = 0; j < 2; ++j) {
+      int tile = wid + j * 4;
+      if (tile >= 5) continue;
+      int col = tile * 16 + lr;
+      float bv = scb[col];
+      #pragma unroll
+      for (int rr = 0; rr < 4; ++rr)
+        scoresOut[(size_t)(m0 + lq * 4 + rr) * 80 + col] = sacc[j][rr] + bv;
+    }
+  }
+}
+
+template<int LQE>
 __launch_bounds__(256)
 __global__ void fdr_kernel(const short* __restrict__ A,
                            const short* __restrict__ W1t, const float* __restrict__ b1,
                            const short* __restrict__ W2t, const float* __restrict__ b2,
                            const short* __restrict__ W3t, const float* __restrict__ b3,
                            const float* __restrict__ cprev, const float* __restrict__ refi,
-                           float* __restrict__ ccur, float* __restrict__ refn) {
+                           float* __restrict__ ccur, float* __restrict__ refn,
+                           const float* __restrict__ scores, const float* __restrict__ lw1,
+                           const float* __restrict__ lb1, const float* __restrict__ lw2,
+                           const float* __restrict__ lb2, float* __restrict__ outp) {
   __shared__ short h1[16][264];
   __shared__ short h2[16][264];
   __shared__ float cor[16][132];
   __shared__ float dstl[16][4];
   __shared__ float projs[33];
+  __shared__ float statl[16][20];
+  __shared__ float interb[16][4];
+  __shared__ float lqes[16];
   const int m0 = blockIdx.x * 16;
   const int tid = threadIdx.x, wid = tid >> 6, lane = tid & 63;
   const int lr = lane & 15, lq = lane >> 4;
@@ -424,10 +547,27 @@
     float m = -1e30f;
     #pragma unroll
     for (int j = 0; j < 33; ++j) m = fmaxf(m, cp[j]);
+    float t0 = -1e30f, t1 = -1e30f, t2v = -1e30f, t3 = -1e30f;
     float sum = 0.f, dot = 0.f;
     #pragma unroll
-    for (int j = 0; j < 33; ++j) { float e = __expf(cp[j] - m); sum += e; dot += e * projs[j]; }
+    for (int j = 0; j < 33; ++j) {
+      float e = __expf(cp[j] - m);
+      sum += e; dot += e * projs[j];
+      if (LQE) {
+        if (e > t0)      { t3 = t2v; t2v = t1; t1 = t0; t0 = e; }
+        else if (e > t1) { t3 = t2v; t2v = t1; t1 = e; }
+        else if (e > t2v){ t3 = t2v; t2v = e; }
+        else if (e > t3) { t3 = e; }
+      }
+    }
     dstl[r][sd] = dot / sum;
+    if (LQE) {
+      float inv = 1.f / sum;
+      float v0 = t0 * inv, v1 = t1 * inv, v2 = t2v * inv, v3 = t3 * inv;
+      statl[r][sd * 5 + 0] = v0; statl[r][sd * 5 + 1] = v1;
+      statl[r][sd * 5 + 2] = v2; statl[r][sd * 5 + 3] = v3;
+      statl[r][sd * 5 + 4] = (v0 + v1 + v2 + v3) * 0.25f;
+    }
   }
   __syncthreads();
   if (tid < 16) {
@@ -438,6 +578,28 @@
     float x2 = px + (2.f + dstl[tid][2]) * qw, y2 = py + (2.f + dstl[tid][3]) * qh;
     float4 o; o.x = (x1 + x2) * 0.5f; o.y = (y1 + y2) * 0.5f; o.z = x2 - x1; o.w = y2 - y1;
     *(float4*)(refn + (size_t)g * 4) = o;
+    if (LQE) { interb[tid][0] = o.x; interb[tid][1] = o.y; interb[tid][2] = o.z; interb[tid][3] = o.w; }
+  }
+  if (LQE) {
+    #pragma unroll
+    for (int it = 0; it < 4; ++it) {
+      int row = wid * 4 + it;
+      float sv = lb1[lane];
+      #pragma unroll
+      for (int i = 0; i < 20; ++i) sv += statl[row][i] * lw1[i * 64 + lane];
+      float hv = sv / (1.f + __expf(-sv));
+      float v = hv * lw2[lane];
+      #pragma unroll
+      for (int o = 32; o; o >>= 1) v += __shfl_xor(v, o);
+      if (lane == 0) lqes[row] = v + lb2[0];
+    }
+    __syncthreads();
+    for (int idx = tid; idx < 16 * 84; idx += 256) {
+      int r = idx / 84, c = idx - r * 84;
+      int g = m0 + r;
+      outp[(size_t)g * 84 + c] = (c < 4) ? interb[r][c]
+                                         : scores[(size_t)g * 80 + (c - 4)] + lqes[r];
+    }
   }
 }
 
@@ -593,52 +755,6 @@
     *(float4*)(output + (size_t)rowg * 256 + c) = vo;
     short4 vs; vs.x = f2bf(v0); vs.y = f2bf(v1); vs.z = f2bf(v2); vs.w = f2bf(v3);
     *(short4*)(outbf + (size_t)rowg * 256 + c) = vs;
-  }
-}
-
-__launch_bounds__(256)
-__global__ void qp_mlp(const float* __restrict__ ref, const float* __restrict__ W1,
-                       const float* __restrict__ b1, const short* __restrict__ W2t,
-                       const float* __restrict__ b2, const float* __restrict__ output,
-                       float* __restrict__ qpout, short* __restrict__ oqbf) {
-  __shared__ short sh[16 * 520];
-  const int m0 = blockIdx.x * 16;
-  const int tid = threadIdx.x;
-  for (int i = tid; i < 16 * 512; i += 256) {
-    int r = i >> 9, n = i & 511;
-    float4 rv = *(const float4*)(ref + (size_t)(m0 + r) * 4);
-    float v = b1[n] + rv.x * W1[n] + rv.y * W1[512 + n] + rv.z * W1[1024 + n]
-            + rv.w * W1[1536 + n];
-    v = v / (1.f + __expf(-v));
-    sh[r * 520 + n] = f2bf(v);
-  }
-  __syncthreads();
-  const int wid = tid >> 6, lane = tid & 63;
-  const int lr = lane & 15, lq = lane >> 4;
-  f32x4 acc[4];
-  #pragma unroll
-  for (int t = 0; t < 4; ++t) acc[t] = (f32x4){0.f, 0.f, 0.f, 0.f};
-  #pragma unroll 4
-  for (int k0 = 0; k0 < 512; k0 += 32) {
-    bf16x8 a = *(const bf16x8*)&sh[lr * 520 + k0 + lq * 8];
-    #pragma unroll
-    for (int t = 0; t < 4; ++t) {
-      bf16x8 w = *(const bf16x8*)(W2t + (size_t)(wid * 64 + t * 16 + lr) * 512 + k0 + lq * 8);
-      acc[t] = __builtin_amdgcn_mfma_f32_16x16x32_bf16(a, w, acc[t], 0, 0, 0);
-    }
-  }
-  #pragma unroll
-  for (int t = 0; t < 4; ++t) {
-    int col = wid * 64 + t * 16 + lr;
-    float bv = b2[col];
-    #pragma unroll
-    for (int rr = 0; rr < 4; ++rr) {
-      int rowg = m0 + lq * 4 + rr;
-      size_t idx = (size_t)rowg * 256 + col;
-      float v = fminf(fmaxf(acc[t][rr] + bv, -10.f), 10.f);
-      qpout[idx] = v;
-      oqbf[idx] = f2bf(v + output[idx]);
-    }
   }
 }
 
@@ -789,107 +905,6 @@
   size_t off = (size_t)row * D_ + h * HD_ + c;
   t2[off] = acc;
   t2bf[off] = f2bf(acc);
-}
-
-__launch_bounds__(64)
-__global__ void lqe_kernel(const float* __restrict__ scores, const float* __restrict__ corners,
-                           const float* __restrict__ w1, const float* __restrict__ b1,
-                           const float* __restrict__ w2, const float* __restrict__ b2,
-                           const float* __restrict__ inter, float* __restrict__ out) {
-  const int row = blockIdx.x;
-  const int tid = threadIdx.x;
-  __shared__ float stat[20];
-  __shared__ float lqe_s;
-  if (tid < 4) {
-    const float* cp = corners + (size_t)row * (4 * NBIN_) + tid * NBIN_;
-    float m = -1e30f;
-    for (int j = 0; j < NBIN_; ++j) m = fmaxf(m, cp[j]);
-    float e[NBIN_]; float sum = 0.f;
-    for (int j = 0; j < NBIN_; ++j) { e[j] = __expf(cp[j] - m); sum += e[j]; }
-    float inv = 1.f / sum;
-    float mean = 0.f;
-    for (int t = 0; t < 4; ++t) {
-      int bi = 0; float best = -1.f;
-      for (int j = 0; j < NBIN_; ++j) if (e[j] > best) { best = e[j]; bi = j; }
-      e[bi] = -2.f;
-      float v = best * inv;
-      stat[tid * 5 + t] = v; mean += v;
-    }
-    stat[tid * 5 + 4] = mean * 0.25f;
-  }
-  __syncthreads();
-  float s = b1[tid];
-  #pragma unroll
-  for (int i = 0; i < 20; ++i) s += stat[i] * w1[i * 64 + tid];
-  float hv = s / (1.f + __expf(-s));
-  float v = hv * w2[tid];
-  #pragma unroll
-  for (int o = 32; o; o >>= 1) v += __shfl_down(v, o);
-  if (tid == 0) lqe_s = v + b2[0];
-  __syncthreads();
-  if (tid < 4) out[(size_t)row * 84 + tid] = inter[row * 4 + tid];
-  for (int c = tid; c < NC_; c += 64)
-    out[(size_t)row * 84 + 4 + c] = scores[(size_t)row * NC_ + c] + lqe_s;
-}
-
-__global__ void fill0_kernel(float* __restrict__ p, int n) {
-  int i = blockIdx.x * 256 + threadIdx.x; if (i < n) p[i] = 0.f;
-}
-__global__ void sigmoid_kernel(float* __restrict__ d, const float* __restrict__ s, int n) {
-  int i = blockIdx.x * 256 + threadIdx.x; if (i < n) d[i] = 1.f / (1.f + __expf(-s[i]));
-}
-__global__ void initcvt_kernel(float* __restrict__ o, short* __restrict__ ob,
-                               const float* __restrict__ t, int n4) {
-  int i = blockIdx.x * 256 + threadIdx.x;
-  if (i < n4) {
-    float4 v = ((const float4*)t)[i];
-    ((float4*)o)[i] = v;
-    short4 s; s.x = f2bf(v.x); s.y = f2bf(v.y); s.z = f2bf(v.z); s.w = f2bf(v.w);
-    ((short4*)ob)[i] = s;
-  }
-}
-__global__ void bcat_kernel(const float* __restrict__ qb, const float* __restrict__ kb,
-                            const float* __restrict__ vb, const float* __restrict__ ob,
-                            const float* __restrict__ ab, float* __restrict__ qkvb,
-                            float* __restrict__ offawb) {
-  int i = blockIdx.x * 256 + threadIdx.x;
-  if (i < NLAYERS_ * 768) {
-    int l = i / 768, c = i % 768;
-    qkvb[i] = (c < 256) ? qb[l * 256 + c] : (c < 512) ? kb[l * 256 + c - 256]
-                        : vb[l * 256 + c - 512];
-  }
-  if (i < NLAYERS_ * 288) {
-    int l = i / 288, c = i % 288;
-    offawb[i] = (c < 192) ? ob[l * 192 + c] : ab[l * 96 + c - 192];
-  }
-}
-
-template<int KT>
-static void launch_bgemm_k(hipStream_t st, const short* A, const short* A2, int N2,
-                           const short* Acat, int KA, const short* Wt, const float* bias,
-                           const float* Cadd, float* Cf, short* Cbf, int M, int N, int act) {
-  dim3 g((N + 63) / 64, M / 64), blk(256);
-  switch (act) {
-    case 0: bgemm<0,KT><<<g, blk, 0, st>>>(A, A2, N2, Acat, KA, Wt, bias, Cadd, Cf, Cbf, M, N); break;
-    case 1: bgemm<1,KT><<<g, blk, 0, st>>>(A, A2, N2, Acat, KA, Wt, bias, Cadd, Cf, Cbf, M, N); break;
-    case 2: bgemm<2,KT><<<g, blk, 0, st>>>(A, A2, N2, Acat, KA, Wt, bias, Cadd, Cf, Cbf, M, N); break;
-    case 3: bgemm<3,KT><<<g, blk, 0, st>>>(A, A2, N2, Acat, KA, Wt, bias, Cadd, Cf, Cbf, M, N); break;
-    case 4: bgemm<4,KT><<<g, blk, 0, st>>>(A, A2, N2, Acat, KA, Wt, bias, Cadd, Cf, Cbf, M, N); break;
-  }
-}
-static void launch_bgemm(hipStream_t st, const short* A, const short* A2, int N2,
-                         const short* Acat, int KA, const short* Wt, const float* bias,
-                         const float* Cadd, float* Cf, short* Cbf,
-                         int M, int N, int K, int act) {
-  if (K == 256)      launch_bgemm_k<256>(st, A, A2, N2, Acat, KA, Wt, bias, Cadd, Cf, Cbf, M, N, act);
-  else if (K == 512) launch_bgemm_k<512>(st, A, A2, N2, Acat, KA, Wt, bias, Cadd, Cf, Cbf, M, N, act);
-  else               launch_bgemm_k<1024>(st, A, A2, N2, Acat, KA, Wt, bias, Cadd, Cf, Cbf, M, N, act);
-}
-
-static void conv_w(hipStream_t st, const float* W, short* Wt, int K, int N, int L,
-                   size_t ostride) {
-  dim3 g((K + 31) / 32, (N + 31) / 32, L);
-  wconv_kernel<<<g, 256, 0, st>>>(W, Wt, K, N, ostride);
 }
 
 static inline dim3 egrid(int n) { return dim3((n + 255) / 256); }
@@ -974,47 +989,51 @@
   float* c_prev = corners0; float* c_cur = corners1;
   float* ref_cur = refA;    float* ref_nxt = refB;
 
-  conv_w(stream, qp_w2, qp2t, 512, 256, 1, 0);
-  conv_w(stream, sa_qw, sqkvt,               256, 256, NLAYERS_, 768 * 256);
-  conv_w(stream, sa_kw, sqkvt + 256 * 256,   256, 256, NLAYERS_, 768 * 256);
-  conv_w(stream, sa_vw, sqkvt + 512 * 256,   256, 256, NLAYERS_, 768 * 256);
-  conv_w(stream, sa_ow, sowt, 256, 256, NLAYERS_, 256 * 256);
-  conv_w(stream, off_w, soffawt,             256, 192, NLAYERS_, 288 * 256);
-  conv_w(stream, aw_w,  soffawt + 192 * 256, 256,  96, NLAYERS_, 288 * 256);
-  conv_w(stream, gate_w, gatet, 512, 512, NLAYERS_, 512 * 512);
-  conv_w(stream, ff1_w, ff1t, 256, 1024, NLAYERS_, 1024 * 256);
-  conv_w(stream, ff2_w, ff2t, 1024, 256, NLAYERS_, 256 * 1024);
-  conv_w(stream, bb_w1, bb1t, 256, 256, NLAYERS_, 256 * 256);
-  conv_w(stream, bb_w2, bb2t, 256, 256, NLAYERS_, 256 * 256);
-  conv_w(stream, bb_w3, bb3t, 256, 132, NLAYERS_, 132 * 256);
-  conv_w(stream, pb_w1, pb1t, 256, 256, 1, 0);
-  conv_w(stream, pb_w2, pb2t, 256, 256, 1, 0);
-  conv_w(stream, pb_w3, pb3t, 256, 4, 1, 0);
-  conv_w(stream, sc_w + (size_t)5 * D_ * NC_, sct, 256, 80, 1, 0);
-  bcat_kernel<<<egrid(NLAYERS_ * 768), 256, 0, stream>>>(sa_qb, sa_kb, sa_vb, off_b, aw_b,
-                                                         qkvb, offawb);
+  WJobs P; int nb = 0; int nj = 0;
+  auto addj = [&](const float* s, short* d2, int K, int N, int L, int ostr) {
+    P.j[nj].src = s; P.j[nj].dst = d2; P.j[nj].K = K; P.j[nj].N = N;
+    P.j[nj].tk = (K + 31) / 32; P.j[nj].tn = (N + 31) / 32;
+    P.j[nj].L = L; P.j[nj].ostride = ostr; P.j[nj].blk0 = nb; P.j[nj].pad = 0;
+    nb += P.j[nj].tk * P.j[nj].tn * L; ++nj;
+  };
+  addj(qp_w2, qp2t, 512, 256, 1, 512 * 256);
+  addj(sa_qw, sqkvt,               256, 256, NLAYERS_, 768 * 256);
+  addj(sa_kw, sqkvt + 256 * 256,   256, 256, NLAYERS_, 768 * 256);
+  addj(sa_vw, sqkvt + 512 * 256,   256, 256, NLAYERS_, 768 * 256);
+  addj(sa_ow, sowt, 256, 256, NLAYERS_, 256 * 256);
+  addj(off_w, soffawt,             256, 192, NLAYERS_, 288 * 256);
+  addj(aw_w,  soffawt + 192 * 256, 256,  96, NLAYERS_, 288 * 256);
+  addj(gate_w, gatet, 512, 512, NLAYERS_, 512 * 512);
+  addj(ff1_w, ff1t, 256, 1024, NLAYERS_, 1024 * 256);
+  addj(ff2_w, ff2t, 1024, 256, NLAYERS_, 256 * 1024);
+  addj(bb_w1, bb1t, 256, 256, NLAYERS_, 256 * 256);
+  addj(bb_w2, bb2t, 256, 256, NLAYERS_, 256 * 256);
+  addj(bb_w3, bb3t, 256, 132, NLAYERS_, 132 * 256);
+  addj(pb_w1, pb1t, 256, 256, 1, 256 * 256);
+  addj(pb_w2, pb2t, 256, 256, 1, 256 * 256);
+  addj(pb_w3, pb3t, 256, 4, 1, 4 * 256);
+  addj(sc_w + (size_t)5 * D_ * NC_, sct, 256, 80, 1, 80 * 256);
+  P.njobs = nj;
+  wconv_all<<<dim3(nb), 256, 0, stream>>>(P);
   if (bf16mem)
     memconv_kernel<<<dim3(B_ * STOT_ / 4), 256, 0, stream>>>(memory, membf);
 
-  fill0_kernel<<<egrid(R_ * D_), 256, 0, stream>>>(out_prev, R_ * D_);
-  fill0_kernel<<<egrid(R_ * 4 * NBIN_), 256, 0, stream>>>(c_prev, R_ * 4 * NBIN_);
-  sigmoid_kernel<<<egrid(R_ * 4), 256, 0, stream>>>(ref_cur, ref_unact, R_ * 4);
-  initcvt_kernel<<<egrid(R_ * D_ / 4), 256, 0, stream>>>(output, outbf, target, R_ * D_ / 4);
+  misc_init<<<egrid(R_ * 64), 256, 0, stream>>>(target, ref_unact,
+      sa_qb, sa_kb, sa_vb, off_b, aw_b,
+      output, outbf, out_prev, c_prev, ref_cur, qkvb, offawb);
 
   for (int i = 0; i < NLAYERS_; ++i) {
-    qp_mlp<<<dim3(300), 256, 0, stream>>>(ref_cur, qp_w1, qp_b1, qp2t, qp_b2,
-                                          output, qp, oqbf);
-
-    launch_bgemm(stream, oqbf, outbf, 512, nullptr, 0, sqkvt + (size_t)i * 768 * 256,
-                 qkvb + (size_t)i * 768, nullptr, nullptr, qkv, R_, 768, 256, 0);
+    qp_qkv<<<dim3(300), 256, 0, stream>>>(ref_cur, qp_w1, qp_b1, qp2t, qp_b2,
+                                          output, outbf,
+                                          sqkvt + (size_t)i * 768 * 256,
+                                          qkvb + (size_t)i * 768, qp, qkv);
     attn3_kernel<<<dim3(B_ * NH_ * 2), 256, 0, stream>>>(qkv, tbf);
-    gemm_ln<256, 0><<<dim3(300), 256, 0, stream>>>(
+    sow_ln_off<<<dim3(300), 256, 0, stream>>>(
         tbf, sowt + (size_t)i * 65536, sa_ob + (size_t)i * D_, output,
-        n1_g + (size_t)i * D_, n1_b + (size_t)i * D_, qp, nullptr,
-        output, outbf, oqbf);
-
-    launch_bgemm(stream, oqbf, nullptr, 0, nullptr, 0, soffawt + (size_t)i * 288 * 256,
-                 offawb + (size_t)i * 288, nullptr, offawf, nullptr, R_, 288, 256, 0);
+        n1_g + (size_t)i * D_, n1_b + (size_t)i * D_, qp,
+        soffawt + (size_t)i * 288 * 256, offawb + (size_t)i * 288,
+        output, outbf, offawf);
+
     if (bf16mem)
       deform_kernel<1><<<dim3(R_), 256, 0, stream>>>(membf, offawf, ref_cur, t2, tbf);
     else
@@ -1025,31 +1044,37 @@
                                            gn_g + (size_t)i * D_, gn_b + (size_t)i * D_,
                                            output, outbf);
 
-    ffn_ln<<<dim3(300), 256, 0, stream>>>(outbf, ff1t + (size_t)i * 262144,
-                                          ff1_b + (size_t)i * FF_,
-                                          ff2t + (size_t)i * 262144, ff2_b + (size_t)i * D_,
-                                          output, n3_g + (size_t)i * D_, n3_b + (size_t)i * D_,
-                                          out_prev, output, outbf, oqbf);
+    if (i < NLAYERS_ - 1)
+      ffn_ln<0><<<dim3(300), 256, 0, stream>>>(outbf, ff1t + (size_t)i * 262144,
+          ff1_b + (size_t)i * FF_, ff2t + (size_t)i * 262144, ff2_b + (size_t)i * D_,
+          output, n3_g + (size_t)i * D_, n3_b + (size_t)i * D_,
+          out_prev, output, outbf, oqbf, nullptr, nullptr, nullptr);
+    else
+      ffn_ln<1><<<dim3(300), 256, 0, stream>>>(outbf, ff1t + (size_t)i * 262144,
+          ff1_b + (size_t)i * FF_, ff2t + (size_t)i * 262144, ff2_b + (size_t)i * D_,
+          output, n3_g + (size_t)i * D_, n3_b + (size_t)i * D_,
+          out_prev, output, outbf, oqbf, sct, sc_b + (size_t)5 * NC_, scores);
 
     if (i == 0)
       pb_fused<<<dim3(300), 256, 0, stream>>>(outbf, pb1t, pb_b1, pb2t, pb_b2,
                                               pb3t, pb_b3, ref_cur, ref_init);
-    fdr_kernel<<<dim3(300), 256, 0, stream>>>(oqbf,
-                                              bb1t + (size_t)i * 65536, bb_b1 + (size_t)i * D_,
-                                              bb2t + (size_t)i * 65536, bb_b2 + (size_t)i * D_,
-                                              bb3t + (size_t)i * 33792, bb_b3 + (size_t)i * 4 * NBIN_,
-                                              c_prev, ref_init, c_cur, ref_nxt);
-
-    if (i == NLAYERS_ - 1) {
-      launch_bgemm(stream, outbf, nullptr, 0, nullptr, 0, sct, sc_b + (size_t)5 * NC_,
-                   nullptr, scores, nullptr, R_, NC_, 256, 0);
-      lqe_kernel<<<dim3(R_), 64, 0, stream>>>(scores, c_cur,
-                                              lqe_w1 + (size_t)5 * 20 * 64, lqe_b1 + (size_t)5 * 64,
-                                              lqe_w2 + (size_t)5 * 64, lqe_b2 + (size_t)5,
-                                              ref_nxt, out);
-    } else {
+    if (i < NLAYERS_ - 1) {
+      fdr_kernel<0><<<dim3(300), 256, 0, stream>>>(oqbf,
+          bb1t + (size_t)i * 65536, bb_b1 + (size_t)i * D_,
+          bb2t + (size_t)i * 65536, bb_b2 + (size_t)i * D_,
+          bb3t + (size_t)i * 33792, bb_b3 + (size_t)i * 4 * NBIN_,
+          c_prev, ref_init, c_cur, ref_nxt,
+          nullptr, nullptr, nullptr, nullptr, nullptr, nullptr);
       std::swap(c_prev, c_cur);
       std::swap(ref_cur, ref_nxt);
-    }
-  }
-}
+    } else {
+      fdr_kernel<1><<<dim3(300), 256, 0, stream>>>(oqbf,
+          bb1t + (size_t)i * 65536, bb_b1 + (size_t)i * D_,
+          bb2t + (size_t)i * 65536, bb_b2 + (size_t)i * D_,
+          bb3t + (size_t)i * 33792, bb_b3 + (size_t)i * 4 * NBIN_,
+          c_prev, ref_init, c_cur, ref_nxt,
+          scores, lqe_w1 + (size_t)5 * 20 * 64, lqe_b1 + (size_t)5 * 64,
+          lqe_w2 + (size_t)5 * 64, lqe_b2 + (size_t)5, out);
+    }
+  }
+}
```

Measured after the change: 1.893 ms. 1.03x faster.
